# Kernel tuning notes

Measured on AMD Instinct MI355X. Metric: run time of the kernel, lower is better.

The kernel has to match this reference:

```python
import jax, jax.numpy as jnp
import numpy as np

B, N, NE = 16, 96, 256
ATOM, EDIM, HID, LAT, HEADS = 128, 16, 128, 128, 4
HD = LAT // HEADS
RBF, CUT, ZEMB, MAXZ = 16, 5.0, 32, 100
MUL0_IN, MUL1_IN = 64, 32      # irreps_node = 64x0e + 32x1o (dim 160)
MUL0_OUT, MUL1_OUT = 32, 16    # out irreps  = 32x0e + 16x1o (dim 80)
NODE_DIM = MUL0_IN + 3 * MUL1_IN
OUT_DIM = MUL0_OUT + 3 * MUL1_OUT
E_ATT = 1024
WNUM = MUL0_IN*MUL0_OUT + MUL0_IN*MUL1_OUT + MUL1_IN*MUL1_OUT + MUL1_IN*MUL0_OUT  # 4608


def _mlp3(x, w1, b1, w2, b2, w3, b3):
    x = jax.nn.silu(x @ w1 + b1)
    x = jax.nn.silu(x @ w2 + b2)
    return x @ w3 + b3


def setup_inputs() -> dict:
    key = jax.random.key(0)
    ks = jax.random.split(key, 40)
    s = 0.05  # scale params so deep MLP activations stay numerically sane
    d = {}
    d['h'] = jax.random.normal(ks[0], (B, N, ATOM), jnp.float32)
    d['h_full'] = jax.random.normal(ks[1], (B, N, NODE_DIM), jnp.float32)
    d['e_feat'] = jax.random.normal(ks[2], (NE, EDIM), jnp.float32)
    d['att_dist'] = jax.random.uniform(ks[3], (E_ATT,), jnp.float32)
    d['att_vec'] = jax.random.normal(ks[4], (E_ATT, 3), jnp.float32)
    d['z_emb_table'] = jax.random.normal(ks[5], (MAXZ + 1, ZEMB), jnp.float32) * s
    d['rw1'] = jax.random.normal(ks[6], (ZEMB + 1 + RBF, HID), jnp.float32) * s
    d['rb1'] = jnp.zeros((HID,), jnp.float32)
    d['rw2'] = jax.random.normal(ks[7], (HID, WNUM), jnp.float32) * s
    d['rb2'] = jnp.zeros((WNUM,), jnp.float32)
    d['ew1'] = jax.random.normal(ks[8], (EDIM, HID), jnp.float32) * s
    d['eb1'] = jnp.zeros((HID,), jnp.float32)
    d['ew2'] = jax.random.normal(ks[9], (HID, MUL0_OUT + MUL1_OUT), jnp.float32) * s
    d['eb2'] = jnp.zeros((MUL0_OUT + MUL1_OUT,), jnp.float32)
    d['qw1'] = jax.random.normal(ks[10], (ATOM + EDIM, HID), jnp.float32) * s
    d['qb1'] = jnp.zeros((HID,), jnp.float32)
    d['qw2'] = jax.random.normal(ks[11], (HID, HID), jnp.float32) * s
    d['qb2'] = jnp.zeros((HID,), jnp.float32)
    d['qw3'] = jax.random.normal(ks[12], (HID, LAT), jnp.float32) * s
    d['qb3'] = jnp.zeros((LAT,), jnp.float32)
    d['kw1'] = jax.random.normal(ks[13], (ATOM + ZEMB + 1 + RBF, HID), jnp.float32) * s
    d['kb1'] = jnp.zeros((HID,), jnp.float32)
    d['kw2'] = jax.random.normal(ks[14], (HID, HID), jnp.float32) * s
    d['kb2'] = jnp.zeros((HID,), jnp.float32)
    d['kw3'] = jax.random.normal(ks[15], (HID, LAT), jnp.float32) * s
    d['kb3'] = jnp.zeros((LAT,), jnp.float32)
    d['ow1'] = jax.random.normal(ks[16], (MUL0_OUT + MUL1_OUT, HID), jnp.float32) * s
    d['ob1'] = jnp.zeros((HID,), jnp.float32)
    d['ow2'] = jax.random.normal(ks[17], (HID, HID), jnp.float32) * s
    d['ob2'] = jnp.zeros((HID,), jnp.float32)
    d['ow3'] = jax.random.normal(ks[18], (HID, LAT), jnp.float32) * s
    d['ob3'] = jnp.zeros((LAT,), jnp.float32)
    d['z'] = jax.random.randint(ks[19], (B, N), 0, MAXZ)
    d['mask'] = jnp.ones((B, N), bool)
    d['absorber_index'] = jax.random.randint(ks[20], (B,), 0, N)
    d['att_dst'] = jnp.arange(E_ATT)  # unique flat indices into B*N
    return d


def reference(h, h_full, e_feat, att_dist, att_vec, z_emb_table,
              rw1, rb1, rw2, rb2, ew1, eb1, ew2, eb2,
              qw1, qb1, qw2, qb2, qw3, qb3,
              kw1, kb1, kw2, kb2, kw3, kb3,
              ow1, ob1, ow2, ob2, ow3, ob3,
              z, mask, absorber_index, att_dst):
    Bz, Na, Hd = h.shape
    F = Bz * Na
    nE = e_feat.shape[0]
    # scatter edge data into flat (B*N) atom slots
    am_flat = jnp.zeros((F,), bool).at[att_dst].set(True)
    d_flat = jnp.zeros((F,), h.dtype).at[att_dst].set(att_dist)
    v_flat = jnp.zeros((F, 3), h.dtype).at[att_dst].set(att_vec)
    att_mask = am_flat.reshape(Bz, Na) & mask
    # spherical harmonics (lmax=1, component normalization): Y0 = 1, Y1 = sqrt(3)*unit_vec
    un = v_flat / jnp.maximum(jnp.linalg.norm(v_flat, axis=-1, keepdims=True), 1e-8)
    y1 = jnp.sqrt(3.0) * un
    # Gaussian RBF on absorber->atom distance
    mu = jnp.linspace(0.0, CUT, RBF)
    delta = CUT / (RBF - 1)
    rbf = jnp.exp(-(d_flat[:, None] - mu) ** 2 / (2.0 * delta * delta))  # (F, RBF)
    zr = z_emb_table[z]                      # (B, N, ZEMB)
    zr_flat = zr.reshape(F, -1)
    is_abs = jnp.zeros((Bz, Na), h.dtype).at[jnp.arange(Bz), absorber_index].set(1.0)
    # radial MLP -> per-edge tensor-product weights
    w_in = jnp.concatenate([zr_flat, is_abs.reshape(F, 1), rbf], -1)
    tpw = jax.nn.silu(w_in @ rw1 + rb1) @ rw2 + rb2  # (F, WNUM)
    s1 = MUL0_IN * MUL0_OUT
    s2 = s1 + MUL0_IN * MUL1_OUT
    s3 = s2 + MUL1_IN * MUL1_OUT
    w00 = tpw[:, :s1].reshape(F, MUL0_IN, MUL0_OUT)   # 0e x 0e -> 0e
    w01 = tpw[:, s1:s2].reshape(F, MUL0_IN, MUL1_OUT) # 0e x 1o -> 1o
    w10 = tpw[:, s2:s3].reshape(F, MUL1_IN, MUL1_OUT) # 1o x 0e -> 1o
    w11 = tpw[:, s3:].reshape(F, MUL1_IN, MUL0_OUT)   # 1o x 1o -> 0e
    hf = h_full.reshape(F, -1)
    x0 = hf[:, :MUL0_IN]
    x1 = hf[:, MUL0_IN:].reshape(F, MUL1_IN, 3)
    alpha = 1.0 / jnp.sqrt(jnp.float32(MUL0_IN + MUL1_IN))  # path fan-in normalization
    c = 1.0 / jnp.sqrt(3.0)                                  # wigner-3j coeff for l=1 couplings
    out0 = alpha * (jnp.einsum('fi,fio->fo', x0, w00)
                    + c * jnp.einsum('fim,fm,fio->fo', x1, y1, w11))
    out1 = alpha * c * (jnp.einsum('fi,fm,fio->fom', x0, y1, w01)
                        + jnp.einsum('fim,fio->fom', x1, w10))
    v_irrep = jnp.concatenate([out0, out1.reshape(F, 3 * MUL1_OUT)], -1)  # (F, OUT_DIM)
    # cosine cutoff envelope + edge mask
    env = jnp.where(d_flat < CUT, 0.5 * (jnp.cos(jnp.pi * d_flat / CUT) + 1.0), 0.0)
    v_irrep = v_irrep * (am_flat.astype(h.dtype) * env)[:, None]
    # energy-conditioned per-irrep-channel modulation
    gates = jax.nn.silu(e_feat @ ew1 + eb1) @ ew2 + eb2  # (nE, 48)
    g_exp = jnp.concatenate([gates[:, :MUL0_OUT],
                             jnp.repeat(gates[:, MUL0_OUT:], 3, axis=-1)], -1)  # (nE, OUT_DIM)
    v_mod = (v_irrep[:, None, :] * g_exp[None]).reshape(Bz, Na, nE, OUT_DIM)
    # invariant multi-head scoring
    h_abs = h[jnp.arange(Bz), absorber_index]  # (B, H)
    q_in = jnp.concatenate([jnp.broadcast_to(h_abs[:, None], (Bz, nE, Hd)),
                            jnp.broadcast_to(e_feat[None], (Bz, nE, EDIM))], -1)
    q = _mlp3(q_in, qw1, qb1, qw2, qb2, qw3, qb3)  # (B, nE, LAT)
    atom_static = jnp.concatenate([h, zr, is_abs[..., None], rbf.reshape(Bz, Na, RBF)], -1)
    k = _mlp3(atom_static, kw1, kb1, kw2, kb2, kw3, kb3)  # (B, N, LAT)
    qh = q.reshape(Bz, nE, HEADS, HD)
    kh = k.reshape(Bz, Na, HEADS, HD)
    scores = (jnp.einsum('behd,bnhd->benh', qh, kh) * (HD ** -0.5)).mean(-1)  # (B, nE, N)
    m = att_mask[:, None, :]
    scores = jnp.where(m, scores, -1e9)
    attn = jax.nn.softmax(scores, axis=2) * m.astype(h.dtype)
    attn = attn / jnp.maximum(attn.sum(2, keepdims=True), 1e-8)
    out_irrep = jnp.einsum('ben,bnec->bec', attn, v_mod)  # (B, nE, OUT_DIM)
    # invariants: scalars + vector norms
    scal = out_irrep[..., :MUL0_OUT]
    vec = out_irrep[..., MUL0_OUT:].reshape(Bz, nE, MUL1_OUT, 3)
    inv = jnp.concatenate([scal, jnp.sqrt(jnp.sum(vec * vec, -1) + 1e-12)], -1)
    return _mlp3(inv, ow1, ob1, ow2, ob2, ow3, ob3)  # (B, nE, LAT)
```

## Files before the change

### kernel.cpp

```cpp
#include <hip/hip_runtime.h>
#include <hip/hip_fp16.h>
#include <math.h>

#define BB 16
#define NN 96
#define NE 256
#define FF (BB*NN)
#define ATOM 128
#define EDIM 16
#define HID 128
#define LAT 128
#define RBFN 16
#define CUTOFF 5.0f
#define ZEMB 32
#define E_ATT 1024
#define M0I 64
#define M1I 32
#define M0O 32
#define M1O 16
#define NODE_DIM 160
#define OUT_DIM 80
#define INVD 48
#define WNUM 4608
#define SEG1 2048
#define SEG2 3072
#define SEG3 3584

#define EDGE_BLKS (E_ATT/4)
#define EC_BLKS 16
#define HABS_BLKS 2
#define GATE_BLKS 16
#define TRANS_BLKS 144
#define PREP_BLKS 1
#define STAGE1_BLKS (EDGE_BLKS + EC_BLKS + HABS_BLKS + GATE_BLKS + TRANS_BLKS + PREP_BLKS)

#define MFMA_BLKS (36*16)
#define MQ_BLKS (MFMA_BLKS + 512)

#define SCORE_BLKS 128
#define ST_BLKS (SCORE_BLKS + 512)

typedef _Float16 half8_t __attribute__((ext_vector_type(8)));
typedef float float4v __attribute__((ext_vector_type(4)));

__device__ __forceinline__ float silu_f(float x) { return x / (1.0f + expf(-x)); }

__global__ __launch_bounds__(256) void k_stage1(
    const float* __restrict__ h, const float* __restrict__ z_emb, const int* __restrict__ z,
    const int* __restrict__ absorber, const float* __restrict__ e_feat,
    const int* __restrict__ att_dst, const float* __restrict__ att_dist,
    const float* __restrict__ att_vec,
    const float* __restrict__ rw1, const float* __restrict__ rb1,
    const float* __restrict__ kw1, const float* __restrict__ kb1,
    const float* __restrict__ kw2, const float* __restrict__ kb2,
    const float* __restrict__ kw3, const float* __restrict__ kb3,
    const float* __restrict__ qw1,
    const float* __restrict__ ew1, const float* __restrict__ eb1,
    const float* __restrict__ ew2, const float* __restrict__ eb2,
    const float* __restrict__ rw2,
    __half* __restrict__ hiddenH, float* __restrict__ kmatw,
    float* __restrict__ ecw, float* __restrict__ habs1w, float* __restrict__ gexp,
    __half* __restrict__ rw2T,
    int* __restrict__ inv, float* __restrict__ y1E, float* __restrict__ envE)
{
    __shared__ float smem[3488];
    int blk = blockIdx.x;
    int t = threadIdx.x;

    if (blk < EDGE_BLKS) {
        float (*sin1)[184] = (float(*)[184])smem;
        float (*l1S)[128]  = (float(*)[128])(smem + 736);
        float (*l2S)[128]  = (float(*)[128])(smem + 736 + 512);
        int w = t >> 6;
        int c = t & 63;
        int e = blk*4 + w;
        int f = att_dst[e];
        int b = f / NN, nn = f - b*NN;
        float d = att_dist[e];
        {
            float2 hv = *(const float2*)&h[f*ATOM + 2*c];
            sin1[w][2*c] = hv.x; sin1[w][2*c + 1] = hv.y;
        }
        if (c < ZEMB) sin1[w][ATOM + c] = z_emb[z[f]*ZEMB + c];
        if (c >= 32 && c < 48) {
            int j = c - 32;
            const float delta = CUTOFF / (RBFN - 1);
            float diff = d - j*delta;
            sin1[w][ATOM + ZEMB + 1 + j] = expf(-diff*diff / (2.0f*delta*delta));
        }
        if (c == 48) sin1[w][ATOM + ZEMB] = (absorber[b] == nn) ? 1.0f : 0.0f;
        __syncthreads();
        int c2 = 2*c;
        {
            float2 a0 = *(const float2*)&rb1[c2];
            float2 a1 = make_float2(0.f, 0.f);
            #pragma unroll 8
            for (int i = 0; i < 48; i += 2) {
                float x0v = sin1[w][ATOM + i], x1v = sin1[w][ATOM + i + 1];
                float2 w0 = *(const float2*)&rw1[i*HID + c2];
                float2 w1 = *(const float2*)&rw1[(i+1)*HID + c2];
                a0.x += x0v*w0.x; a0.y += x0v*w0.y;
                a1.x += x1v*w1.x; a1.y += x1v*w1.y;
            }
            {
                float x0v = sin1[w][ATOM + 48];
                float2 w0 = *(const float2*)&rw1[48*HID + c2];
                a0.x += x0v*w0.x; a0.y += x0v*w0.y;
            }
            *(__half2*)&hiddenH[e*HID + c2] =
                __floats2half2_rn(silu_f(a0.x + a1.x), silu_f(a0.y + a1.y));
        }
        {
            float2 a0 = *(const float2*)&kb1[c2];
            float2 a1 = make_float2(0.f, 0.f);
            #pragma unroll 8
            for (int i = 0; i < 176; i += 2) {
                float x0v = sin1[w][i], x1v = sin1[w][i + 1];
                float2 w0 = *(const float2*)&kw1[i*HID + c2];
                float2 w1 = *(const float2*)&kw1[(i+1)*HID + c2];
                a0.x += x0v*w0.x; a0.y += x0v*w0.y;
                a1.x += x1v*w1.x; a1.y += x1v*w1.y;
            }
            {
                float x0v = sin1[w][176];
                float2 w0 = *(const float2*)&kw1[176*HID + c2];
                a0.x += x0v*w0.x; a0.y += x0v*w0.y;
            }
            l1S[w][c2] = silu_f(a0.x + a1.x); l1S[w][c2+1] = silu_f(a0.y + a1.y);
        }
        __syncthreads();
        {
            float2 a0 = *(const float2*)&kb2[c2];
            float2 a1 = make_float2(0.f, 0.f);
            #pragma unroll 8
            for (int i = 0; i < HID; i += 2) {
                float x0v = l1S[w][i], x1v = l1S[w][i + 1];
                float2 w0 = *(const float2*)&kw2[i*HID + c2];
                float2 w1 = *(const float2*)&kw2[(i+1)*HID + c2];
                a0.x += x0v*w0.x; a0.y += x0v*w0.y;
                a1.x += x1v*w1.x; a1.y += x1v*w1.y;
            }
            l2S[w][c2] = silu_f(a0.x + a1.x); l2S[w][c2+1] = silu_f(a0.y + a1.y);
        }
        __syncthreads();
        {
            float2 a0 = *(const float2*)&kb3[c2];
            float2 a1 = make_float2(0.f, 0.f);
            #pragma unroll 8
            for (int i = 0; i < HID; i += 2) {
                float x0v = l2S[w][i], x1v = l2S[w][i + 1];
                float2 w0 = *(const float2*)&kw3[i*HID + c2];
                float2 w1 = *(const float2*)&kw3[(i+1)*HID + c2];
                a0.x += x0v*w0.x; a0.y += x0v*w0.y;
                a1.x += x1v*w1.x; a1.y += x1v*w1.y;
            }
            float2 o; o.x = a0.x + a1.x; o.y = a0.y + a1.y;
            *(float2*)&kmatw[f*HID + c2] = o;
        }
    } else if (blk < EDGE_BLKS + EC_BLKS) {
        float (*ef)[16] = (float(*)[16])smem;
        int e0 = (blk - EDGE_BLKS) * 16;
        { int e = t >> 4, i = t & 15; ef[e][i] = e_feat[(e0 + e)*EDIM + i]; }
        __syncthreads();
        int r = t >> 4, c0 = (t & 15)*8;
        float4 a0 = make_float4(0,0,0,0), a1 = a0;
        #pragma unroll
        for (int i = 0; i < EDIM; i++) {
            float a = ef[r][i];
            float4 w0 = *(const float4*)&qw1[(ATOM + i)*HID + c0];
            float4 w1 = *(const float4*)&qw1[(ATOM + i)*HID + c0 + 4];
            a0.x += a*w0.x; a0.y += a*w0.y; a0.z += a*w0.z; a0.w += a*w0.w;
            a1.x += a*w1.x; a1.y += a*w1.y; a1.z += a*w1.z; a1.w += a*w1.w;
        }
        *(float4*)&ecw[(e0 + r)*HID + c0] = a0;
        *(float4*)&ecw[(e0 + r)*HID + c0 + 4] = a1;
    } else if (blk < EDGE_BLKS + EC_BLKS + HABS_BLKS) {
        float (*hr)[128] = (float(*)[128])smem;
        int b0 = (blk - EDGE_BLKS - EC_BLKS) * 8;
        {
            int r = t >> 5, i4 = t & 31;
            int b = b0 + r;
            int a = absorber[b];
            *(float4*)&hr[r][i4*4] = *(const float4*)&h[(b*NN + a)*ATOM + i4*4];
        }
        __syncthreads();
        int r = t >> 5, c0 = (t & 31)*4;
        float4 a0 = make_float4(0,0,0,0), a1 = a0;
        #pragma unroll 8
        for (int i = 0; i < ATOM; i += 2) {
            float x0v = hr[r][i], x1v = hr[r][i+1];
            float4 w0 = *(const float4*)&qw1[i*HID + c0];
            float4 w1 = *(const float4*)&qw1[(i+1)*HID + c0];
            a0.x += x0v*w0.x; a0.y += x0v*w0.y; a0.z += x0v*w0.z; a0.w += x0v*w0.w;
            a1.x += x1v*w1.x; a1.y += x1v*w1.y; a1.z += x1v*w1.z; a1.w += x1v*w1.w;
        }
        float4 o;
        o.x = a0.x + a1.x; o.y = a0.y + a1.y; o.z = a0.z + a1.z; o.w = a0.w + a1.w;
        *(float4*)&habs1w[(b0 + r)*HID + c0] = o;
    } else if (blk < EDGE_BLKS + EC_BLKS + HABS_BLKS + GATE_BLKS) {
        float (*ef)[16]   = (float(*)[16])smem;
        float (*l1g)[128] = (float(*)[128])(smem + 256);
        float (*gg)[48]   = (float(*)[48])(smem + 256 + 2048);
        int e0 = (blk - EDGE_BLKS - EC_BLKS - HABS_BLKS) * 16;
        { int e = t >> 4, i = t & 15; ef[e][i] = e_feat[(e0 + e)*EDIM + i]; }
        __syncthreads();
        int r = t >> 4, c0 = (t & 15)*8;
        {
            float4 a0 = *(const float4*)&eb1[c0];
            float4 a1 = *(const float4*)&eb1[c0 + 4];
            #pragma unroll
            for (int i = 0; i < EDIM; i++) {
                float a = ef[r][i];
                float4 w0 = *(const float4*)&ew1[i*HID + c0];
                float4 w1 = *(const float4*)&ew1[i*HID + c0 + 4];
                a0.x += a*w0.x; a0.y += a*w0.y; a0.z += a*w0.z; a0.w += a*w0.w;
                a1.x += a*w1.x; a1.y += a*w1.y; a1.z += a*w1.z; a1.w += a*w1.w;
            }
            l1g[r][c0]   = silu_f(a0.x); l1g[r][c0+1] = silu_f(a0.y);
            l1g[r][c0+2] = silu_f(a0.z); l1g[r][c0+3] = silu_f(a0.w);
            l1g[r][c0+4] = silu_f(a1.x); l1g[r][c0+5] = silu_f(a1.y);
            l1g[r][c0+6] = silu_f(a1.z); l1g[r][c0+7] = silu_f(a1.w);
        }
        __syncthreads();
        for (int u = t; u < 16*48; u += 256) {
            int e = u / 48, j = u - 48*(u/48);
            float acc = eb2[j];
            #pragma unroll 4
            for (int i = 0; i < HID; i++) acc += l1g[e][i]*ew2[i*48 + j];
            gg[e][j] = acc;
        }
        __syncthreads();
        for (int u = t; u < 16*80; u += 256) {
            int e = u / 80, cc = u - 80*(u/80);
            gexp[(e0 + e)*OUT_DIM + cc] = (cc < M0O) ? gg[e][cc] : gg[e][M0O + (cc - M0O)/3];
        }
    } else if (blk < EDGE_BLKS + EC_BLKS + HABS_BLKS + GATE_BLKS + TRANS_BLKS) {
        __half* lds = (__half*)smem;
        int tb = blk - (EDGE_BLKS + EC_BLKS + HABS_BLKS + GATE_BLKS);
        int nt = tb % 72, kt = tb / 72;
        int n0 = nt*64, k0 = kt*64;
        for (int p = 0; p < 16; p++) {
            int idx = t + 256*p;
            int kk = idx >> 6, nn = idx & 63;
            lds[nn*66 + kk] = __float2half(rw2[(k0+kk)*WNUM + n0+nn]);
        }
        __syncthreads();
        for (int p = 0; p < 16; p++) {
            int idx = t + 256*p;
            int nn = idx >> 6, kk = idx & 63;
            rw2T[(n0+nn)*HID + k0+kk] = lds[nn*66 + kk];
        }
    } else {
        for (int p = 0; p < 6; p++) inv[t + 256*p] = -1;
        for (int p = 0; p < 4; p++) {
            int e = t + 256*p;
            float d = att_dist[e];
            envE[e] = (d < CUTOFF) ? 0.5f*(cosf(3.14159265358979323846f*d/CUTOFF) + 1.0f) : 0.0f;
            float vx = att_vec[3*e], vy = att_vec[3*e+1], vz = att_vec[3*e+2];
            float nrm = sqrtf(vx*vx + vy*vy + vz*vz);
            float is = 1.0f / fmaxf(nrm, 1e-8f);
            const float s3 = 1.7320508075688772f;
            y1E[3*e]   = s3*vx*is;
            y1E[3*e+1] = s3*vy*is;
            y1E[3*e+2] = s3*vz*is;
        }
        __syncthreads();
        for (int p = 0; p < 4; p++) { int e = t + 256*p; inv[att_dst[e]] = e; }
    }
}

__global__ __launch_bounds__(256) void k_mq(
    const __half* __restrict__ hiddenH, const __half* __restrict__ rw2T,
    const float* __restrict__ rb2,
    const float* __restrict__ habs1, const float* __restrict__ ec, const float* __restrict__ qb1,
    const float* __restrict__ qw2, const float* __restrict__ qb2,
    const float* __restrict__ qw3, const float* __restrict__ qb3,
    __half* __restrict__ tpwE, float* __restrict__ qmat)
{
    __shared__ __align__(16) char smemraw[17408];
    int blk = blockIdx.x;
    int t = threadIdx.x;
    if (blk < MFMA_BLKS) {
        int colTile = blk % 36;
        int rowGrp  = blk / 36;
        int wv = t >> 6;
        int lane = t & 63;
        int m0 = (rowGrp*4 + wv) * 16;
        int n0 = colTile * 128;
        int mrow = lane & 15, quad = lane >> 4;
        __half* cS = (__half*)smemraw + wv * (16*136);
        const _Float16* hp = (const _Float16*)hiddenH + (m0 + mrow)*HID + quad*8;
        half8_t af[4];
        #pragma unroll
        for (int kc = 0; kc < 4; kc++) af[kc] = *(const half8_t*)(hp + kc*32);
        #pragma unroll
        for (int nt = 0; nt < 8; nt++) {
            const _Float16* bp = (const _Float16*)rw2T + (n0 + nt*16 + mrow)*HID + quad*8;
            float4v acc = {0.f, 0.f, 0.f, 0.f};
            #pragma unroll
            for (int kc = 0; kc < 4; kc++) {
                half8_t bf = *(const half8_t*)(bp + kc*32);
                acc = __builtin_amdgcn_mfma_f32_16x16x32_f16(af[kc], bf, acc, 0, 0, 0);
            }
            float bias = rb2[n0 + nt*16 + mrow];
            #pragma unroll
            for (int r = 0; r < 4; r++)
                cS[(quad*4 + r)*136 + nt*16 + mrow] = __float2half(acc[r] + bias);
        }
        #pragma unroll
        for (int p = 0; p < 4; p++) {
            int chunk = lane + 64*p;
            int row = chunk >> 4, c8 = (chunk & 15)*8;
            float4 v = *(float4*)&cS[row*136 + c8];
            *(float4*)&tpwE[(long)(m0 + row)*WNUM + n0 + c8] = v;
        }
    } else {
        float* l1S = (float*)smemraw;
        float* l2S = (float*)smemraw + 1024;
        int r0 = (blk - MFMA_BLKS) * 8;
        for (int p = 0; p < 4; p++) {
            int idx = t + 256*p;
            int rr = idx >> 7, i = idx & 127;
            int be = r0 + rr; int b = be >> 8; int e = be & 255;
            l1S[rr*128 + i] = silu_f(habs1[b*HID + i] + ec[e*HID + i] + qb1[i]);
        }
        __syncthreads();
        int r = t >> 5, c0 = (t & 31)*4;
        {
            float4 a0 = *(const float4*)&qb2[c0];
            float4 a1 = make_float4(0,0,0,0);
            #pragma unroll 8
            for (int i = 0; i < HID; i += 2) {
                float x0v = l1S[r*128 + i], x1v = l1S[r*128 + i+1];
                float4 w0 = *(const float4*)&qw2[i*HID + c0];
                float4 w1 = *(const float4*)&qw2[(i+1)*HID + c0];
                a0.x += x0v*w0.x; a0.y += x0v*w0.y; a0.z += x0v*w0.z; a0.w += x0v*w0.w;
                a1.x += x1v*w1.x; a1.y += x1v*w1.y; a1.z += x1v*w1.z; a1.w += x1v*w1.w;
            }
            l2S[r*128 + c0]   = silu_f(a0.x + a1.x); l2S[r*128 + c0+1] = silu_f(a0.y + a1.y);
            l2S[r*128 + c0+2] = silu_f(a0.z + a1.z); l2S[r*128 + c0+3] = silu_f(a0.w + a1.w);
        }
        __syncthreads();
        {
            float4 a0 = *(const float4*)&qb3[c0];
            float4 a1 = make_float4(0,0,0,0);
            #pragma unroll 8
            for (int i = 0; i < HID; i += 2) {
                float x0v = l2S[r*128 + i], x1v = l2S[r*128 + i+1];
                float4 w0 = *(const float4*)&qw3[i*HID + c0];
                float4 w1 = *(const float4*)&qw3[(i+1)*HID + c0];
                a0.x += x0v*w0.x; a0.y += x0v*w0.y; a0.z += x0v*w0.z; a0.w += x0v*w0.w;
                a1.x += x1v*w1.x; a1.y += x1v*w1.y; a1.z += x1v*w1.z; a1.w += x1v*w1.w;
            }
            float4 o;
            o.x = a0.x + a1.x; o.y = a0.y + a1.y; o.z = a0.z + a1.z; o.w = a0.w + a1.w;
            *(float4*)&qmat[(r0 + r)*LAT + c0] = o;
        }
    }
}

__global__ __launch_bounds__(256) void k_st(
    const float* __restrict__ qmat, const float* __restrict__ kmat, const int* __restrict__ inv,
    const float* __restrict__ h_full, const __half* __restrict__ tpwE,
    const int* __restrict__ att_dst,
    const float* __restrict__ envE, const float* __restrict__ y1E,
    float* __restrict__ scoresW, float* __restrict__ virr)
{
    __shared__ float smem[8544];
    int blk = blockIdx.x;
    int t = threadIdx.x;
    if (blk < SCORE_BLKS) {
        int b  = blk >> 3;
        int e0 = (blk & 7) * 32;
        float (*Qs)[132] = (float(*)[132])smem;
        float (*Kt)[132] = (float(*)[132])(smem + 32*132);
        float* mS = smem + 2*32*132;
        for (int p = 0; p < 4; p++) {
            int idx = t + 256*p; int e = idx >> 5, i4 = idx & 31;
            *(float4*)&Qs[e][i4*4] = *(const float4*)&qmat[(b*NE + e0 + e)*LAT + i4*4];
        }
        if (t < NN) mS[t] = ((unsigned)inv[b*NN + t] < E_ATT) ? 1.0f : 0.0f;
        int te = t >> 5, tn = t & 31;
        float acc[4][3] = {};
        for (int nt = 0; nt < 3; nt++) {
            __syncthreads();
            for (int p = 0; p < 4; p++) {
                int idx = t + 256*p; int n = idx >> 5, i4 = idx & 31;
                *(float4*)&Kt[n][i4*4] = *(const float4*)&kmat[(b*NN + nt*32 + n)*LAT + i4*4];
            }
            __syncthreads();
            for (int i = 0; i < LAT; i++) {
                float bv = Kt[tn][i];
                acc[0][nt] += Qs[te*4 + 0][i]*bv;
                acc[1][nt] += Qs[te*4 + 1][i]*bv;
                acc[2][nt] += Qs[te*4 + 2][i]*bv;
                acc[3][nt] += Qs[te*4 + 3][i]*bv;
            }
        }
        const float scale = 0.04419417382415922f;
        #pragma unroll
        for (int j = 0; j < 4; j++)
            #pragma unroll
            for (int jj = 0; jj < 3; jj++) {
                int n = tn + 32*jj;
                float s = (mS[n] != 0.f) ? acc[j][jj]*scale : -1e9f;
                scoresW[((b*NE) + e0 + te*4 + j)*NN + n] = s;
            }
    } else {
        int sub = t >> 7, tt = t & 127;
        int e = (blk - SCORE_BLKS)*2 + sub;
        int f = att_dst[e];
        float* x0  = smem + sub*256;
        float* x1f = smem + sub*256 + 64;
        float* xy  = smem + sub*256 + 160;
        float* y1s = smem + sub*256 + 192;
        const float* hf = h_full + f*NODE_DIM;
        if (tt < M0I) x0[tt] = hf[tt];
        if (tt < M1I*3) x1f[tt] = hf[M0I + tt];
        if (tt < 3) y1s[tt] = y1E[3*e + tt];
        __syncthreads();
        if (tt < M1I) xy[tt] = x1f[3*tt]*y1s[0] + x1f[3*tt+1]*y1s[1] + x1f[3*tt+2]*y1s[2];
        __syncthreads();
        float scale = envE[e];
        const __half* w = tpwE + (long)e*WNUM;
        const float alpha = 0.10206207261596575f;
        const float cc = 0.5773502691896258f;
        if (tt < M0O) {
            float t00 = 0.f, t11 = 0.f;
            #pragma unroll 4
            for (int i = 0; i < M0I; i++) t00 += x0[i]*__half2float(w[i*M0O + tt]);
            #pragma unroll 4
            for (int i = 0; i < M1I; i++) t11 += xy[i]*__half2float(w[SEG3 + i*M0O + tt]);
            virr[f*OUT_DIM + tt] = alpha*(t00 + cc*t11)*scale;
        } else if (tt < M0O + 3*M1O) {
            int idx = tt - M0O; int o = idx/3, m = idx - 3*o;
            float t01 = 0.f, t10 = 0.f;
            #pragma unroll 4
            for (int i = 0; i < M0I; i++) t01 += x0[i]*__half2float(w[SEG1 + i*M1O + o]);
            #pragma unroll 4
            for (int i = 0; i < M1I; i++) t10 += x1f[i*3 + m]*__half2float(w[SEG2 + i*M1O + o]);
            virr[f*OUT_DIM + tt] = alpha*cc*(t01*y1s[m] + t10)*scale;
        }
    }
}

__global__ __launch_bounds__(256) void k_attf(
    const float* __restrict__ scoresW, const int* __restrict__ inv,
    const float* __restrict__ virr, const float* __restrict__ gexp,
    const float* __restrict__ ow1, const float* __restrict__ ob1,
    const float* __restrict__ ow2, const float* __restrict__ ob2,
    const float* __restrict__ ow3, const float* __restrict__ ob3,
    float* __restrict__ out)
{
    int b  = blockIdx.x >> 5;
    int e0 = (blockIdx.x & 31) * 8;
    int t = threadIdx.x;
    __shared__ float aS[8][100];
    __shared__ float gS[8][84];
    __shared__ float ocS[8][84];
    __shared__ float mS[NN];
    __shared__ float inS[8][INVD];
    __shared__ float l1S[8][HID];
    __shared__ float l2S[8][HID];

    for (int p = 0; p < 3; p++) {
        int idx = t + 256*p;
        int el = idx / NN, n = idx - NN*(idx/NN);
        aS[el][n] = scoresW[((b*NE) + e0 + el)*NN + n];
    }
    if (t < 160) {
        int el = t / 20, c4 = t - 20*(t/20);
        *(float4*)&gS[el][c4*4] = *(const float4*)&gexp[(e0 + el)*OUT_DIM + c4*4];
    }
    if (t < NN) mS[t] = ((unsigned)inv[b*NN + t] < E_ATT) ? 1.0f : 0.0f;
    __syncthreads();

    {
        int el = t >> 5;
        int ng = t & 31;
        float s0 = aS[el][ng], s1 = aS[el][ng + 32], s2 = aS[el][ng + 64];
        float m0 = mS[ng], m1 = mS[ng + 32], m2 = mS[ng + 64];
        float mx = fmaxf(s0, fmaxf(s1, s2));
        #pragma unroll
        for (int off = 1; off < 32; off <<= 1) mx = fmaxf(mx, __shfl_xor(mx, off));
        float e0v = expf(s0 - mx), e1v = expf(s1 - mx), e2v = expf(s2 - mx);
        float sm = e0v + e1v + e2v;
        #pragma unroll
        for (int off = 1; off < 32; off <<= 1) sm += __shfl_xor(sm, off);
        float r = 1.0f / sm;
        float p0 = m0*e0v*r, p1 = m1*e1v*r, p2 = m2*e2v*r;
        float ss = p0 + p1 + p2;
        #pragma unroll
        for (int off = 1; off < 32; off <<= 1) ss += __shfl_xor(ss, off);
        float is = 1.0f / fmaxf(ss, 1e-8f);
        aS[el][ng]      = p0*is;
        aS[el][ng + 32] = p1*is;
        aS[el][ng + 64] = p2*is;
    }
    __syncthreads();

    if (t < 160) {
        int el = t / 20, c4 = t - 20*(t/20);
        const float* vp = virr + (long)b*NN*OUT_DIM + c4*4;
        float4 acc = make_float4(0,0,0,0);
        #pragma unroll 4
        for (int n = 0; n < NN; n++) {
            float a = aS[el][n];
            float4 v = *(const float4*)&vp[n*OUT_DIM];
            acc.x += a*v.x; acc.y += a*v.y; acc.z += a*v.z; acc.w += a*v.w;
        }
        float4 g = *(float4*)&gS[el][c4*4];
        float4 o; o.x = acc.x*g.x; o.y = acc.y*g.y; o.z = acc.z*g.z; o.w = acc.w*g.w;
        *(float4*)&ocS[el][c4*4] = o;
    }
    __syncthreads();

    for (int u = t; u < 8*INVD; u += 256) {
        int el = u / INVD, j = u - INVD*(u/INVD);
        float val;
        if (j < M0O) val = ocS[el][j];
        else {
            int o = j - M0O;
            float x = ocS[el][M0O + 3*o], y = ocS[el][M0O + 3*o + 1], zz = ocS[el][M0O + 3*o + 2];
            val = sqrtf(x*x + y*y + zz*zz + 1e-12f);
        }
        inS[el][j] = val;
    }
    __syncthreads();

    int r = t >> 5, c0 = (t & 31)*4;
    {
        float4 a0 = *(const float4*)&ob1[c0];
        float4 a1 = make_float4(0,0,0,0);
        #pragma unroll 8
        for (int i = 0; i < INVD; i += 2) {
            float x0v = inS[r][i], x1v = inS[r][i+1];
            float4 w0 = *(const float4*)&ow1[i*HID + c0];
            float4 w1 = *(const float4*)&ow1[(i+1)*HID + c0];
            a0.x += x0v*w0.x; a0.y += x0v*w0.y; a0.z += x0v*w0.z; a0.w += x0v*w0.w;
            a1.x += x1v*w1.x; a1.y += x1v*w1.y; a1.z += x1v*w1.z; a1.w += x1v*w1.w;
        }
        l1S[r][c0]   = silu_f(a0.x + a1.x); l1S[r][c0+1] = silu_f(a0.y + a1.y);
        l1S[r][c0+2] = silu_f(a0.z + a1.z); l1S[r][c0+3] = silu_f(a0.w + a1.w);
    }
    __syncthreads();
    {
        float4 a0 = *(const float4*)&ob2[c0];
        float4 a1 = make_float4(0,0,0,0);
        #pragma unroll 8
        for (int i = 0; i < HID; i += 2) {
            float x0v = l1S[r][i], x1v = l1S[r][i+1];
            float4 w0 = *(const float4*)&ow2[i*HID + c0];
            float4 w1 = *(const float4*)&ow2[(i+1)*HID + c0];
            a0.x += x0v*w0.x; a0.y += x0v*w0.y; a0.z += x0v*w0.z; a0.w += x0v*w0.w;
            a1.x += x1v*w1.x; a1.y += x1v*w1.y; a1.z += x1v*w1.z; a1.w += x1v*w1.w;
        }
        l2S[r][c0]   = silu_f(a0.x + a1.x); l2S[r][c0+1] = silu_f(a0.y + a1.y);
        l2S[r][c0+2] = silu_f(a0.z + a1.z); l2S[r][c0+3] = silu_f(a0.w + a1.w);
    }
    __syncthreads();
    {
        float4 a0 = *(const float4*)&ob3[c0];
        float4 a1 = make_float4(0,0,0,0);
        #pragma unroll 8
        for (int i = 0; i < HID; i += 2) {
            float x0v = l2S[r][i], x1v = l2S[r][i+1];
            float4 w0 = *(const float4*)&ow3[i*HID + c0];
            float4 w1 = *(const float4*)&ow3[(i+1)*HID + c0];
            a0.x += x0v*w0.x; a0.y += x0v*w0.y; a0.z += x0v*w0.z; a0.w += x0v*w0.w;
            a1.x += x1v*w1.x; a1.y += x1v*w1.y; a1.z += x1v*w1.z; a1.w += x1v*w1.w;
        }
        float4 o;
        o.x = a0.x + a1.x; o.y = a0.y + a1.y; o.z = a0.z + a1.z; o.w = a0.w + a1.w;
        *(float4*)&out[((b*NE + e0) + r)*LAT + c0] = o;
    }
}

extern "C" void kernel_launch(void* const* d_in, const int* in_sizes, int n_in,
                              void* d_out, int out_size, void* d_ws, size_t ws_size,
                              hipStream_t stream) {
    const float* h        = (const float*)d_in[0];
    const float* h_full   = (const float*)d_in[1];
    const float* e_feat   = (const float*)d_in[2];
    const float* att_dist = (const float*)d_in[3];
    const float* att_vec  = (const float*)d_in[4];
    const float* z_emb    = (const float*)d_in[5];
    const float* rw1 = (const float*)d_in[6];  const float* rb1 = (const float*)d_in[7];
    const float* rw2 = (const float*)d_in[8];  const float* rb2 = (const float*)d_in[9];
    const float* ew1 = (const float*)d_in[10]; const float* eb1 = (const float*)d_in[11];
    const float* ew2 = (const float*)d_in[12]; const float* eb2 = (const float*)d_in[13];
    const float* qw1 = (const float*)d_in[14]; const float* qb1 = (const float*)d_in[15];
    const float* qw2 = (const float*)d_in[16]; const float* qb2 = (const float*)d_in[17];
    const float* qw3 = (const float*)d_in[18]; const float* qb3 = (const float*)d_in[19];
    const float* kw1 = (const float*)d_in[20]; const float* kb1 = (const float*)d_in[21];
    const float* kw2 = (const float*)d_in[22]; const float* kb2 = (const float*)d_in[23];
    const float* kw3 = (const float*)d_in[24]; const float* kb3 = (const float*)d_in[25];
    const float* ow1 = (const float*)d_in[26]; const float* ob1 = (const float*)d_in[27];
    const float* ow2 = (const float*)d_in[28]; const float* ob2 = (const float*)d_in[29];
    const float* ow3 = (const float*)d_in[30]; const float* ob3 = (const float*)d_in[31];
    const int* z        = (const int*)d_in[32];
    const int* absorber = (const int*)d_in[34];
    const int* att_dst  = (const int*)d_in[35];

    float* ws = (float*)d_ws;
    int*   inv     = (int*)ws;
    float* y1E     = ws + 1536;
    float* envE    = ws + 4608;
    float* kmat    = ws + 5632;
    float* qmat    = ws + 202240;
    float* gexp    = ws + 726528;
    float* virr    = ws + 747008;
    float* habs1   = ws + 869888;
    float* ec      = ws + 871936;
    float* scoresW = ws + 904704;
    __half* tpwE   = (__half*)(ws + 1297920);
    __half* rw2T   = (__half*)(ws + 3657216);
    __half* hiddenH= (__half*)(ws + 3952128);

    float* out = (float*)d_out;

    k_stage1<<<STAGE1_BLKS, 256, 0, stream>>>(h, z_emb, z, absorber, e_feat,
                                              att_dst, att_dist, att_vec,
                                              rw1, rb1, kw1, kb1, kw2, kb2, kw3, kb3,
                                              qw1, ew1, eb1, ew2, eb2, rw2,
                                              hiddenH, kmat, ec, habs1, gexp, rw2T,
                                              inv, y1E, envE);
    k_mq<<<MQ_BLKS, 256, 0, stream>>>(hiddenH, rw2T, rb2, habs1, ec, qb1,
                                      qw2, qb2, qw3, qb3, tpwE, qmat);
    k_st<<<ST_BLKS, 256, 0, stream>>>(qmat, kmat, inv, h_full, tpwE, att_dst,
                                      envE, y1E, scoresW, virr);
    k_attf<<<BB*32, 256, 0, stream>>>(scoresW, inv, virr, gexp,
                                      ow1, ob1, ow2, ob2, ow3, ob3, out);
}
```

Measured before the change: 237.5 us.

## Fuse four stage kernels into one persistent kernel with grid barriers

Replaces the four separate kernel launches with a single persistent kernel of 512 blocks. Each block loops over the work units of each former stage, and stages are separated by an atomic-counter grid barrier, with a tiny init kernel resetting the counter. The intent is to remove inter-kernel launch gaps and tail drain between the stages. In exchange it relies on all 512 blocks being co-resident (launch_bounds 256,2 plus about 34 KB of shared memory), which risks deadlock if they are not, and it adds spin-wait barrier overhead and possibly lower per-block occupancy.

Result: slower. 494.0 us (+108.0%).

```diff
diff --git a/kernel.cpp b/kernel.cpp
--- a/kernel.cpp
+++ b/kernel.cpp
@@ -31,604 +31,639 @@
 #define HABS_BLKS 2
 #define GATE_BLKS 16
 #define TRANS_BLKS 144
-#define PREP_BLKS 1
-#define STAGE1_BLKS (EDGE_BLKS + EC_BLKS + HABS_BLKS + GATE_BLKS + TRANS_BLKS + PREP_BLKS)
-
-#define MFMA_BLKS (36*16)
-#define MQ_BLKS (MFMA_BLKS + 512)
-
-#define SCORE_BLKS 128
-#define ST_BLKS (SCORE_BLKS + 512)
+#define STAGE1_UNITS (EDGE_BLKS + EC_BLKS + HABS_BLKS + GATE_BLKS + TRANS_BLKS + 1)
+
+#define MFMA_UNITS (36*16)
+#define MQ_UNITS (MFMA_UNITS + 512)
+
+#define SCORE_UNITS 128
+#define ST_UNITS (SCORE_UNITS + 512)
+
+#define ATT_UNITS 512
+
+#define GRID_BLKS 512
+#define SMEM_BYTES 34304
 
 typedef _Float16 half8_t __attribute__((ext_vector_type(8)));
 typedef float float4v __attribute__((ext_vector_type(4)));
 
 __device__ __forceinline__ float silu_f(float x) { return x / (1.0f + expf(-x)); }
 
-__global__ __launch_bounds__(256) void k_stage1(
-    const float* __restrict__ h, const float* __restrict__ z_emb, const int* __restrict__ z,
-    const int* __restrict__ absorber, const float* __restrict__ e_feat,
-    const int* __restrict__ att_dst, const float* __restrict__ att_dist,
-    const float* __restrict__ att_vec,
-    const float* __restrict__ rw1, const float* __restrict__ rb1,
-    const float* __restrict__ kw1, const float* __restrict__ kb1,
-    const float* __restrict__ kw2, const float* __restrict__ kb2,
-    const float* __restrict__ kw3, const float* __restrict__ kb3,
-    const float* __restrict__ qw1,
-    const float* __restrict__ ew1, const float* __restrict__ eb1,
-    const float* __restrict__ ew2, const float* __restrict__ eb2,
-    const float* __restrict__ rw2,
-    __half* __restrict__ hiddenH, float* __restrict__ kmatw,
-    float* __restrict__ ecw, float* __restrict__ habs1w, float* __restrict__ gexp,
-    __half* __restrict__ rw2T,
-    int* __restrict__ inv, float* __restrict__ y1E, float* __restrict__ envE)
+__device__ __forceinline__ void grid_barrier(int* cnt, int target) {
+    __syncthreads();
+    if (threadIdx.x == 0) {
+        __threadfence();
+        atomicAdd(cnt, 1);
+        while (__hip_atomic_load(cnt, __ATOMIC_RELAXED, __HIP_MEMORY_SCOPE_AGENT) < target) {
+            __builtin_amdgcn_s_sleep(2);
+        }
+    }
+    __syncthreads();
+    __threadfence();
+}
+
+struct Params {
+    const float *h, *h_full, *e_feat, *att_dist, *att_vec, *z_emb;
+    const float *rw1, *rb1, *rw2, *rb2;
+    const float *ew1, *eb1, *ew2, *eb2;
+    const float *qw1, *qb1, *qw2, *qb2, *qw3, *qb3;
+    const float *kw1, *kb1, *kw2, *kb2, *kw3, *kb3;
+    const float *ow1, *ob1, *ow2, *ob2, *ow3, *ob3;
+    const int *z, *absorber, *att_dst;
+    __half *hiddenH; float *kmat; float *ec; float *habs1; float *gexp;
+    __half *rw2T; int *inv; float *y1E; float *envE;
+    float *qmat; float *scoresW; __half *tpwE; float *virr;
+    int *bar;
+    float *out;
+};
+
+__global__ void k_init(int* bar) {
+    if (threadIdx.x == 0) bar[0] = 0;
+}
+
+__global__ __launch_bounds__(256, 2) void k_mega(Params p)
 {
-    __shared__ float smem[3488];
-    int blk = blockIdx.x;
-    int t = threadIdx.x;
-
-    if (blk < EDGE_BLKS) {
-        float (*sin1)[184] = (float(*)[184])smem;
-        float (*l1S)[128]  = (float(*)[128])(smem + 736);
-        float (*l2S)[128]  = (float(*)[128])(smem + 736 + 512);
-        int w = t >> 6;
-        int c = t & 63;
-        int e = blk*4 + w;
-        int f = att_dst[e];
-        int b = f / NN, nn = f - b*NN;
-        float d = att_dist[e];
-        {
-            float2 hv = *(const float2*)&h[f*ATOM + 2*c];
-            sin1[w][2*c] = hv.x; sin1[w][2*c + 1] = hv.y;
-        }
-        if (c < ZEMB) sin1[w][ATOM + c] = z_emb[z[f]*ZEMB + c];
-        if (c >= 32 && c < 48) {
-            int j = c - 32;
-            const float delta = CUTOFF / (RBFN - 1);
-            float diff = d - j*delta;
-            sin1[w][ATOM + ZEMB + 1 + j] = expf(-diff*diff / (2.0f*delta*delta));
-        }
-        if (c == 48) sin1[w][ATOM + ZEMB] = (absorber[b] == nn) ? 1.0f : 0.0f;
-        __syncthreads();
-        int c2 = 2*c;
-        {
-            float2 a0 = *(const float2*)&rb1[c2];
-            float2 a1 = make_float2(0.f, 0.f);
-            #pragma unroll 8
-            for (int i = 0; i < 48; i += 2) {
-                float x0v = sin1[w][ATOM + i], x1v = sin1[w][ATOM + i + 1];
-                float2 w0 = *(const float2*)&rw1[i*HID + c2];
-                float2 w1 = *(const float2*)&rw1[(i+1)*HID + c2];
-                a0.x += x0v*w0.x; a0.y += x0v*w0.y;
-                a1.x += x1v*w1.x; a1.y += x1v*w1.y;
-            }
-            {
-                float x0v = sin1[w][ATOM + 48];
-                float2 w0 = *(const float2*)&rw1[48*HID + c2];
-                a0.x += x0v*w0.x; a0.y += x0v*w0.y;
-            }
-            *(__half2*)&hiddenH[e*HID + c2] =
-                __floats2half2_rn(silu_f(a0.x + a1.x), silu_f(a0.y + a1.y));
-        }
-        {
-            float2 a0 = *(const float2*)&kb1[c2];
-            float2 a1 = make_float2(0.f, 0.f);
-            #pragma unroll 8
-            for (int i = 0; i < 176; i += 2) {
-                float x0v = sin1[w][i], x1v = sin1[w][i + 1];
-                float2 w0 = *(const float2*)&kw1[i*HID + c2];
-                float2 w1 = *(const float2*)&kw1[(i+1)*HID + c2];
-                a0.x += x0v*w0.x; a0.y += x0v*w0.y;
-                a1.x += x1v*w1.x; a1.y += x1v*w1.y;
-            }
-            {
-                float x0v = sin1[w][176];
-                float2 w0 = *(const float2*)&kw1[176*HID + c2];
-                a0.x += x0v*w0.x; a0.y += x0v*w0.y;
-            }
-            l1S[w][c2] = silu_f(a0.x + a1.x); l1S[w][c2+1] = silu_f(a0.y + a1.y);
-        }
-        __syncthreads();
-        {
-            float2 a0 = *(const float2*)&kb2[c2];
-            float2 a1 = make_float2(0.f, 0.f);
-            #pragma unroll 8
-            for (int i = 0; i < HID; i += 2) {
-                float x0v = l1S[w][i], x1v = l1S[w][i + 1];
-                float2 w0 = *(const float2*)&kw2[i*HID + c2];
-                float2 w1 = *(const float2*)&kw2[(i+1)*HID + c2];
-                a0.x += x0v*w0.x; a0.y += x0v*w0.y;
-                a1.x += x1v*w1.x; a1.y += x1v*w1.y;
-            }
-            l2S[w][c2] = silu_f(a0.x + a1.x); l2S[w][c2+1] = silu_f(a0.y + a1.y);
-        }
-        __syncthreads();
-        {
-            float2 a0 = *(const float2*)&kb3[c2];
-            float2 a1 = make_float2(0.f, 0.f);
-            #pragma unroll 8
-            for (int i = 0; i < HID; i += 2) {
-                float x0v = l2S[w][i], x1v = l2S[w][i + 1];
-                float2 w0 = *(const float2*)&kw3[i*HID + c2];
-                float2 w1 = *(const float2*)&kw3[(i+1)*HID + c2];
-                a0.x += x0v*w0.x; a0.y += x0v*w0.y;
-                a1.x += x1v*w1.x; a1.y += x1v*w1.y;
-            }
-            float2 o; o.x = a0.x + a1.x; o.y = a0.y + a1.y;
-            *(float2*)&kmatw[f*HID + c2] = o;
-        }
-    } else if (blk < EDGE_BLKS + EC_BLKS) {
-        float (*ef)[16] = (float(*)[16])smem;
-        int e0 = (blk - EDGE_BLKS) * 16;
-        { int e = t >> 4, i = t & 15; ef[e][i] = e_feat[(e0 + e)*EDIM + i]; }
-        __syncthreads();
-        int r = t >> 4, c0 = (t & 15)*8;
-        float4 a0 = make_float4(0,0,0,0), a1 = a0;
-        #pragma unroll
-        for (int i = 0; i < EDIM; i++) {
-            float a = ef[r][i];
-            float4 w0 = *(const float4*)&qw1[(ATOM + i)*HID + c0];
-            float4 w1 = *(const float4*)&qw1[(ATOM + i)*HID + c0 + 4];
-            a0.x += a*w0.x; a0.y += a*w0.y; a0.z += a*w0.z; a0.w += a*w0.w;
-            a1.x += a*w1.x; a1.y += a*w1.y; a1.z += a*w1.z; a1.w += a*w1.w;
-        }
-        *(float4*)&ecw[(e0 + r)*HID + c0] = a0;
-        *(float4*)&ecw[(e0 + r)*HID + c0 + 4] = a1;
-    } else if (blk < EDGE_BLKS + EC_BLKS + HABS_BLKS) {
-        float (*hr)[128] = (float(*)[128])smem;
-        int b0 = (blk - EDGE_BLKS - EC_BLKS) * 8;
-        {
-            int r = t >> 5, i4 = t & 31;
-            int b = b0 + r;
-            int a = absorber[b];
-            *(float4*)&hr[r][i4*4] = *(const float4*)&h[(b*NN + a)*ATOM + i4*4];
-        }
-        __syncthreads();
-        int r = t >> 5, c0 = (t & 31)*4;
-        float4 a0 = make_float4(0,0,0,0), a1 = a0;
-        #pragma unroll 8
-        for (int i = 0; i < ATOM; i += 2) {
-            float x0v = hr[r][i], x1v = hr[r][i+1];
-            float4 w0 = *(const float4*)&qw1[i*HID + c0];
-            float4 w1 = *(const float4*)&qw1[(i+1)*HID + c0];
-            a0.x += x0v*w0.x; a0.y += x0v*w0.y; a0.z += x0v*w0.z; a0.w += x0v*w0.w;
-            a1.x += x1v*w1.x; a1.y += x1v*w1.y; a1.z += x1v*w1.z; a1.w += x1v*w1.w;
-        }
-        float4 o;
-        o.x = a0.x + a1.x; o.y = a0.y + a1.y; o.z = a0.z + a1.z; o.w = a0.w + a1.w;
-        *(float4*)&habs1w[(b0 + r)*HID + c0] = o;
-    } else if (blk < EDGE_BLKS + EC_BLKS + HABS_BLKS + GATE_BLKS) {
-        float (*ef)[16]   = (float(*)[16])smem;
-        float (*l1g)[128] = (float(*)[128])(smem + 256);
-        float (*gg)[48]   = (float(*)[48])(smem + 256 + 2048);
-        int e0 = (blk - EDGE_BLKS - EC_BLKS - HABS_BLKS) * 16;
-        { int e = t >> 4, i = t & 15; ef[e][i] = e_feat[(e0 + e)*EDIM + i]; }
-        __syncthreads();
-        int r = t >> 4, c0 = (t & 15)*8;
-        {
-            float4 a0 = *(const float4*)&eb1[c0];
-            float4 a1 = *(const float4*)&eb1[c0 + 4];
+    __shared__ __align__(16) char smemraw[SMEM_BYTES];
+    float* smem = (float*)smemraw;
+    const int t = threadIdx.x;
+    const int blk = blockIdx.x;
+
+    const float* __restrict__ h        = p.h;
+    const float* __restrict__ h_full   = p.h_full;
+    const float* __restrict__ e_feat   = p.e_feat;
+    const float* __restrict__ att_dist = p.att_dist;
+    const float* __restrict__ att_vec  = p.att_vec;
+    const float* __restrict__ z_emb    = p.z_emb;
+    const float* __restrict__ rw1 = p.rw1; const float* __restrict__ rb1 = p.rb1;
+    const float* __restrict__ rw2 = p.rw2; const float* __restrict__ rb2 = p.rb2;
+    const float* __restrict__ ew1 = p.ew1; const float* __restrict__ eb1 = p.eb1;
+    const float* __restrict__ ew2 = p.ew2; const float* __restrict__ eb2 = p.eb2;
+    const float* __restrict__ qw1 = p.qw1; const float* __restrict__ qb1 = p.qb1;
+    const float* __restrict__ qw2 = p.qw2; const float* __restrict__ qb2 = p.qb2;
+    const float* __restrict__ qw3 = p.qw3; const float* __restrict__ qb3 = p.qb3;
+    const float* __restrict__ kw1 = p.kw1; const float* __restrict__ kb1 = p.kb1;
+    const float* __restrict__ kw2 = p.kw2; const float* __restrict__ kb2 = p.kb2;
+    const float* __restrict__ kw3 = p.kw3; const float* __restrict__ kb3 = p.kb3;
+    const float* __restrict__ ow1 = p.ow1; const float* __restrict__ ob1 = p.ob1;
+    const float* __restrict__ ow2 = p.ow2; const float* __restrict__ ob2 = p.ob2;
+    const float* __restrict__ ow3 = p.ow3; const float* __restrict__ ob3 = p.ob3;
+    const int* __restrict__ z        = p.z;
+    const int* __restrict__ absorber = p.absorber;
+    const int* __restrict__ att_dst  = p.att_dst;
+    __half* __restrict__ hiddenH = p.hiddenH;
+    float*  __restrict__ kmat    = p.kmat;
+    float*  __restrict__ ec      = p.ec;
+    float*  __restrict__ habs1   = p.habs1;
+    float*  __restrict__ gexp    = p.gexp;
+    __half* __restrict__ rw2T    = p.rw2T;
+    int*    __restrict__ inv     = p.inv;
+    float*  __restrict__ y1E     = p.y1E;
+    float*  __restrict__ envE    = p.envE;
+    float*  __restrict__ qmat    = p.qmat;
+    float*  __restrict__ scoresW = p.scoresW;
+    __half* __restrict__ tpwE    = p.tpwE;
+    float*  __restrict__ virr    = p.virr;
+    float*  __restrict__ out     = p.out;
+    int* bar = p.bar;
+
+    for (int u = blk; u < STAGE1_UNITS; u += GRID_BLKS) {
+        if (u < EDGE_BLKS) {
+            float (*sin1)[184] = (float(*)[184])smem;
+            float (*l1S)[128]  = (float(*)[128])(smem + 736);
+            float (*l2S)[128]  = (float(*)[128])(smem + 736 + 512);
+            int w = t >> 6;
+            int c = t & 63;
+            int e = u*4 + w;
+            int f = att_dst[e];
+            int b = f / NN, nn = f - b*NN;
+            float d = att_dist[e];
+            {
+                float2 hv = *(const float2*)&h[f*ATOM + 2*c];
+                sin1[w][2*c] = hv.x; sin1[w][2*c + 1] = hv.y;
+            }
+            if (c < ZEMB) sin1[w][ATOM + c] = z_emb[z[f]*ZEMB + c];
+            if (c >= 32 && c < 48) {
+                int j = c - 32;
+                const float delta = CUTOFF / (RBFN - 1);
+                float diff = d - j*delta;
+                sin1[w][ATOM + ZEMB + 1 + j] = expf(-diff*diff / (2.0f*delta*delta));
+            }
+            if (c == 48) sin1[w][ATOM + ZEMB] = (absorber[b] == nn) ? 1.0f : 0.0f;
+            __syncthreads();
+            int c2 = 2*c;
+            {
+                float2 a0 = *(const float2*)&rb1[c2];
+                float2 a1 = make_float2(0.f, 0.f);
+                #pragma unroll 8
+                for (int i = 0; i < 48; i += 2) {
+                    float x0v = sin1[w][ATOM + i], x1v = sin1[w][ATOM + i + 1];
+                    float2 w0 = *(const float2*)&rw1[i*HID + c2];
+                    float2 w1 = *(const float2*)&rw1[(i+1)*HID + c2];
+                    a0.x += x0v*w0.x; a0.y += x0v*w0.y;
+                    a1.x += x1v*w1.x; a1.y += x1v*w1.y;
+                }
+                {
+                    float x0v = sin1[w][ATOM + 48];
+                    float2 w0 = *(const float2*)&rw1[48*HID + c2];
+                    a0.x += x0v*w0.x; a0.y += x0v*w0.y;
+                }
+                *(__half2*)&hiddenH[e*HID + c2] =
+                    __floats2half2_rn(silu_f(a0.x + a1.x), silu_f(a0.y + a1.y));
+            }
+            {
+                float2 a0 = *(const float2*)&kb1[c2];
+                float2 a1 = make_float2(0.f, 0.f);
+                #pragma unroll 8
+                for (int i = 0; i < 176; i += 2) {
+                    float x0v = sin1[w][i], x1v = sin1[w][i + 1];
+                    float2 w0 = *(const float2*)&kw1[i*HID + c2];
+                    float2 w1 = *(const float2*)&kw1[(i+1)*HID + c2];
+                    a0.x += x0v*w0.x; a0.y += x0v*w0.y;
+                    a1.x += x1v*w1.x; a1.y += x1v*w1.y;
+                }
+                {
+                    float x0v = sin1[w][176];
+                    float2 w0 = *(const float2*)&kw1[176*HID + c2];
+                    a0.x += x0v*w0.x; a0.y += x0v*w0.y;
+                }
+                l1S[w][c2] = silu_f(a0.x + a1.x); l1S[w][c2+1] = silu_f(a0.y + a1.y);
+            }
+            __syncthreads();
+            {
+                float2 a0 = *(const float2*)&kb2[c2];
+                float2 a1 = make_float2(0.f, 0.f);
+                #pragma unroll 8
+                for (int i = 0; i < HID; i += 2) {
+                    float x0v = l1S[w][i], x1v = l1S[w][i + 1];
+                    float2 w0 = *(const float2*)&kw2[i*HID + c2];
+                    float2 w1 = *(const float2*)&kw2[(i+1)*HID + c2];
+                    a0.x += x0v*w0.x; a0.y += x0v*w0.y;
+                    a1.x += x1v*w1.x; a1.y += x1v*w1.y;
+                }
+                l2S[w][c2] = silu_f(a0.x + a1.x); l2S[w][c2+1] = silu_f(a0.y + a1.y);
+            }
+            __syncthreads();
+            {
+                float2 a0 = *(const float2*)&kb3[c2];
+                float2 a1 = make_float2(0.f, 0.f);
+                #pragma unroll 8
+                for (int i = 0; i < HID; i += 2) {
+                    float x0v = l2S[w][i], x1v = l2S[w][i + 1];
+                    float2 w0 = *(const float2*)&kw3[i*HID + c2];
+                    float2 w1 = *(const float2*)&kw3[(i+1)*HID + c2];
+                    a0.x += x0v*w0.x; a0.y += x0v*w0.y;
+                    a1.x += x1v*w1.x; a1.y += x1v*w1.y;
+                }
+                float2 o; o.x = a0.x + a1.x; o.y = a0.y + a1.y;
+                *(float2*)&kmat[f*HID + c2] = o;
+            }
+        } else if (u < EDGE_BLKS + EC_BLKS) {
+            float (*ef)[16] = (float(*)[16])smem;
+            int e0 = (u - EDGE_BLKS) * 16;
+            { int e = t >> 4, i = t & 15; ef[e][i] = e_feat[(e0 + e)*EDIM + i]; }
+            __syncthreads();
+            int r = t >> 4, c0 = (t & 15)*8;
+            float4 a0 = make_float4(0,0,0,0), a1 = a0;
             #pragma unroll
             for (int i = 0; i < EDIM; i++) {
                 float a = ef[r][i];
-                float4 w0 = *(const float4*)&ew1[i*HID + c0];
-                float4 w1 = *(const float4*)&ew1[i*HID + c0 + 4];
+                float4 w0 = *(const float4*)&qw1[(ATOM + i)*HID + c0];
+                float4 w1 = *(const float4*)&qw1[(ATOM + i)*HID + c0 + 4];
                 a0.x += a*w0.x; a0.y += a*w0.y; a0.z += a*w0.z; a0.w += a*w0.w;
                 a1.x += a*w1.x; a1.y += a*w1.y; a1.z += a*w1.z; a1.w += a*w1.w;
             }
-            l1g[r][c0]   = silu_f(a0.x); l1g[r][c0+1] = silu_f(a0.y);
-            l1g[r][c0+2] = silu_f(a0.z); l1g[r][c0+3] = silu_f(a0.w);
-            l1g[r][c0+4] = silu_f(a1.x); l1g[r][c0+5] = silu_f(a1.y);
-            l1g[r][c0+6] = silu_f(a1.z); l1g[r][c0+7] = silu_f(a1.w);
-        }
-        __syncthreads();
-        for (int u = t; u < 16*48; u += 256) {
-            int e = u / 48, j = u - 48*(u/48);
-            float acc = eb2[j];
+            *(float4*)&ec[(e0 + r)*HID + c0] = a0;
+            *(float4*)&ec[(e0 + r)*HID + c0 + 4] = a1;
+        } else if (u < EDGE_BLKS + EC_BLKS + HABS_BLKS) {
+            float (*hr)[128] = (float(*)[128])smem;
+            int b0 = (u - EDGE_BLKS - EC_BLKS) * 8;
+            {
+                int r = t >> 5, i4 = t & 31;
+                int b = b0 + r;
+                int a = absorber[b];
+                *(float4*)&hr[r][i4*4] = *(const float4*)&h[(b*NN + a)*ATOM + i4*4];
+            }
+            __syncthreads();
+            int r = t >> 5, c0 = (t & 31)*4;
+            float4 a0 = make_float4(0,0,0,0), a1 = a0;
+            #pragma unroll 8
+            for (int i = 0; i < ATOM; i += 2) {
+                float x0v = hr[r][i], x1v = hr[r][i+1];
+                float4 w0 = *(const float4*)&qw1[i*HID + c0];
+                float4 w1 = *(const float4*)&qw1[(i+1)*HID + c0];
+                a0.x += x0v*w0.x; a0.y += x0v*w0.y; a0.z += x0v*w0.z; a0.w += x0v*w0.w;
+                a1.x += x1v*w1.x; a1.y += x1v*w1.y; a1.z += x1v*w1.z; a1.w += x1v*w1.w;
+            }
+            float4 o;
+            o.x = a0.x + a1.x; o.y = a0.y + a1.y; o.z = a0.z + a1.z; o.w = a0.w + a1.w;
+            *(float4*)&habs1[(b0 + r)*HID + c0] = o;
+        } else if (u < EDGE_BLKS + EC_BLKS + HABS_BLKS + GATE_BLKS) {
+            float (*ef)[16]   = (float(*)[16])smem;
+            float (*l1g)[128] = (float(*)[128])(smem + 256);
+            float (*gg)[48]   = (float(*)[48])(smem + 256 + 2048);
+            int e0 = (u - EDGE_BLKS - EC_BLKS - HABS_BLKS) * 16;
+            { int e = t >> 4, i = t & 15; ef[e][i] = e_feat[(e0 + e)*EDIM + i]; }
+            __syncthreads();
+            int r = t >> 4, c0 = (t & 15)*8;
+            {
+                float4 a0 = *(const float4*)&eb1[c0];
+                float4 a1 = *(const float4*)&eb1[c0 + 4];
+                #pragma unroll
+                for (int i = 0; i < EDIM; i++) {
+                    float a = ef[r][i];
+                    float4 w0 = *(const float4*)&ew1[i*HID + c0];
+                    float4 w1 = *(const float4*)&ew1[i*HID + c0 + 4];
+                    a0.x += a*w0.x; a0.y += a*w0.y; a0.z += a*w0.z; a0.w += a*w0.w;
+                    a1.x += a*w1.x; a1.y += a*w1.y; a1.z += a*w1.z; a1.w += a*w1.w;
+                }
+                l1g[r][c0]   = silu_f(a0.x); l1g[r][c0+1] = silu_f(a0.y);
+                l1g[r][c0+2] = silu_f(a0.z); l1g[r][c0+3] = silu_f(a0.w);
+                l1g[r][c0+4] = silu_f(a1.x); l1g[r][c0+5] = silu_f(a1.y);
+                l1g[r][c0+6] = silu_f(a1.z); l1g[r][c0+7] = silu_f(a1.w);
+            }
+            __syncthreads();
+            for (int uu = t; uu < 16*48; uu += 256) {
+                int e = uu / 48, j = uu - 48*(uu/48);
+                float acc = eb2[j];
+                #pragma unroll 4
+                for (int i = 0; i < HID; i++) acc += l1g[e][i]*ew2[i*48 + j];
+                gg[e][j] = acc;
+            }
+            __syncthreads();
+            for (int uu = t; uu < 16*80; uu += 256) {
+                int e = uu / 80, cc = uu - 80*(uu/80);
+                gexp[(e0 + e)*OUT_DIM + cc] = (cc < M0O) ? gg[e][cc] : gg[e][M0O + (cc - M0O)/3];
+            }
+        } else if (u < EDGE_BLKS + EC_BLKS + HABS_BLKS + GATE_BLKS + TRANS_BLKS) {
+            __half* lds = (__half*)smem;
+            int tb = u - (EDGE_BLKS + EC_BLKS + HABS_BLKS + GATE_BLKS);
+            int nt = tb % 72, kt = tb / 72;
+            int n0 = nt*64, k0 = kt*64;
+            for (int pp = 0; pp < 16; pp++) {
+                int idx = t + 256*pp;
+                int kk = idx >> 6, nn = idx & 63;
+                lds[nn*66 + kk] = __float2half(rw2[(k0+kk)*WNUM + n0+nn]);
+            }
+            __syncthreads();
+            for (int pp = 0; pp < 16; pp++) {
+                int idx = t + 256*pp;
+                int nn = idx >> 6, kk = idx & 63;
+                rw2T[(n0+nn)*HID + k0+kk] = lds[nn*66 + kk];
+            }
+        } else {
+            for (int pp = 0; pp < 6; pp++) inv[t + 256*pp] = -1;
+            for (int pp = 0; pp < 4; pp++) {
+                int e = t + 256*pp;
+                float d = att_dist[e];
+                envE[e] = (d < CUTOFF) ? 0.5f*(cosf(3.14159265358979323846f*d/CUTOFF) + 1.0f) : 0.0f;
+                float vx = att_vec[3*e], vy = att_vec[3*e+1], vz = att_vec[3*e+2];
+                float nrm = sqrtf(vx*vx + vy*vy + vz*vz);
+                float is = 1.0f / fmaxf(nrm, 1e-8f);
+                const float s3 = 1.7320508075688772f;
+                y1E[3*e]   = s3*vx*is;
+                y1E[3*e+1] = s3*vy*is;
+                y1E[3*e+2] = s3*vz*is;
+            }
+            __syncthreads();
+            for (int pp = 0; pp < 4; pp++) { int e = t + 256*pp; inv[att_dst[e]] = e; }
+        }
+    }
+
+    grid_barrier(bar, GRID_BLKS*1);
+
+    for (int u = blk; u < MQ_UNITS; u += GRID_BLKS) {
+        __syncthreads();
+        if (u < MFMA_UNITS) {
+            int colTile = u % 36;
+            int rowGrp  = u / 36;
+            int wv = t >> 6;
+            int lane = t & 63;
+            int m0 = (rowGrp*4 + wv) * 16;
+            int n0 = colTile * 128;
+            int mrow = lane & 15, quad = lane >> 4;
+            __half* cS = (__half*)smemraw + wv * (16*136);
+            const _Float16* hp = (const _Float16*)hiddenH + (m0 + mrow)*HID + quad*8;
+            half8_t af[4];
+            #pragma unroll
+            for (int kc = 0; kc < 4; kc++) af[kc] = *(const half8_t*)(hp + kc*32);
+            #pragma unroll
+            for (int nt = 0; nt < 8; nt++) {
+                const _Float16* bp = (const _Float16*)rw2T + (n0 + nt*16 + mrow)*HID + quad*8;
+                float4v acc = {0.f, 0.f, 0.f, 0.f};
+                #pragma unroll
+                for (int kc = 0; kc < 4; kc++) {
+                    half8_t bf = *(const half8_t*)(bp + kc*32);
+                    acc = __builtin_amdgcn_mfma_f32_16x16x32_f16(af[kc], bf, acc, 0, 0, 0);
+                }
+                float bias = rb2[n0 + nt*16 + mrow];
+                #pragma unroll
+                for (int r = 0; r < 4; r++)
+                    cS[(quad*4 + r)*136 + nt*16 + mrow] = __float2half(acc[r] + bias);
+            }
+            __syncthreads();
+            #pragma unroll
+            for (int pp = 0; pp < 4; pp++) {
+                int chunk = lane + 64*pp;
+                int row = chunk >> 4, c8 = (chunk & 15)*8;
+                float4 v = *(float4*)&cS[row*136 + c8];
+                *(float4*)&tpwE[(long)(m0 + row)*WNUM + n0 + c8] = v;
+            }
+        } else {
+            float* l1S = smem;
+            float* l2S = smem + 1024;
+            int r0 = (u - MFMA_UNITS) * 8;
+            for (int pp = 0; pp < 4; pp++) {
+                int idx = t + 256*pp;
+                int rr = idx >> 7, i = idx & 127;
+                int be = r0 + rr; int b = be >> 8; int e = be & 255;
+                l1S[rr*128 + i] = silu_f(habs1[b*HID + i] + ec[e*HID + i] + qb1[i]);
+            }
+            __syncthreads();
+            int r = t >> 5, c0 = (t & 31)*4;
+            {
+                float4 a0 = *(const float4*)&qb2[c0];
+                float4 a1 = make_float4(0,0,0,0);
+                #pragma unroll 8
+                for (int i = 0; i < HID; i += 2) {
+                    float x0v = l1S[r*128 + i], x1v = l1S[r*128 + i+1];
+                    float4 w0 = *(const float4*)&qw2[i*HID + c0];
+                    float4 w1 = *(const float4*)&qw2[(i+1)*HID + c0];
+                    a0.x += x0v*w0.x; a0.y += x0v*w0.y; a0.z += x0v*w0.z; a0.w += x0v*w0.w;
+                    a1.x += x1v*w1.x; a1.y += x1v*w1.y; a1.z += x1v*w1.z; a1.w += x1v*w1.w;
+                }
+                l2S[r*128 + c0]   = silu_f(a0.x + a1.x); l2S[r*128 + c0+1] = silu_f(a0.y + a1.y);
+                l2S[r*128 + c0+2] = silu_f(a0.z + a1.z); l2S[r*128 + c0+3] = silu_f(a0.w + a1.w);
+            }
+            __syncthreads();
+            {
+                float4 a0 = *(const float4*)&qb3[c0];
+                float4 a1 = make_float4(0,0,0,0);
+                #pragma unroll 8
+                for (int i = 0; i < HID; i += 2) {
+                    float x0v = l2S[r*128 + i], x1v = l2S[r*128 + i+1];
+                    float4 w0 = *(const float4*)&qw3[i*HID + c0];
+                    float4 w1 = *(const float4*)&qw3[(i+1)*HID + c0];
+                    a0.x += x0v*w0.x; a0.y += x0v*w0.y; a0.z += x0v*w0.z; a0.w += x0v*w0.w;
+                    a1.x += x1v*w1.x; a1.y += x1v*w1.y; a1.z += x1v*w1.z; a1.w += x1v*w1.w;
+                }
+                float4 o;
+                o.x = a0.x + a1.x; o.y = a0.y + a1.y; o.z = a0.z + a1.z; o.w = a0.w + a1.w;
+                *(float4*)&qmat[(r0 + r)*LAT + c0] = o;
+            }
+        }
+    }
+
+    grid_barrier(bar, GRID_BLKS*2);
+
+    for (int u = blk; u < ST_UNITS; u += GRID_BLKS) {
+        __syncthreads();
+        if (u < SCORE_UNITS) {
+            int b  = u >> 3;
+            int e0 = (u & 7) * 32;
+            float (*Qs)[132] = (float(*)[132])smem;
+            float (*Kt)[132] = (float(*)[132])(smem + 32*132);
+            float* mS = smem + 2*32*132;
+            for (int pp = 0; pp < 4; pp++) {
+                int idx = t + 256*pp; int e = idx >> 5, i4 = idx & 31;
+                *(float4*)&Qs[e][i4*4] = *(const float4*)&qmat[(b*NE + e0 + e)*LAT + i4*4];
+            }
+            if (t < NN) mS[t] = ((unsigned)inv[b*NN + t] < E_ATT) ? 1.0f : 0.0f;
+            int te = t >> 5, tn = t & 31;
+            float acc[4][3] = {};
+            for (int nt = 0; nt < 3; nt++) {
+                __syncthreads();
+                for (int pp = 0; pp < 4; pp++) {
+                    int idx = t + 256*pp; int n = idx >> 5, i4 = idx & 31;
+                    *(float4*)&Kt[n][i4*4] = *(const float4*)&kmat[(b*NN + nt*32 + n)*LAT + i4*4];
+                }
+                __syncthreads();
+                for (int i = 0; i < LAT; i++) {
+                    float bv = Kt[tn][i];
+                    acc[0][nt] += Qs[te*4 + 0][i]*bv;
+                    acc[1][nt] += Qs[te*4 + 1][i]*bv;
+                    acc[2][nt] += Qs[te*4 + 2][i]*bv;
+                    acc[3][nt] += Qs[te*4 + 3][i]*bv;
+                }
+            }
+            const float scale = 0.04419417382415922f;
+            #pragma unroll
+            for (int j = 0; j < 4; j++)
+                #pragma unroll
+                for (int jj = 0; jj < 3; jj++) {
+                    int n = tn + 32*jj;
+                    float s = (mS[n] != 0.f) ? acc[j][jj]*scale : -1e9f;
+                    scoresW[((b*NE) + e0 + te*4 + j)*NN + n] = s;
+                }
+        } else {
+            int sub = t >> 7, tt = t & 127;
+            int e = (u - SCORE_UNITS)*2 + sub;
+            int f = att_dst[e];
+            float* x0  = smem + sub*256;
+            float* x1f = smem + sub*256 + 64;
+            float* xy  = smem + sub*256 + 160;
+            float* y1s = smem + sub*256 + 192;
+            const float* hf = h_full + f*NODE_DIM;
+            if (tt < M0I) x0[tt] = hf[tt];
+            if (tt < M1I*3) x1f[tt] = hf[M0I + tt];
+            if (tt < 3) y1s[tt] = y1E[3*e + tt];
+            __syncthreads();
+            if (tt < M1I) xy[tt] = x1f[3*tt]*y1s[0] + x1f[3*tt+1]*y1s[1] + x1f[3*tt+2]*y1s[2];
+            __syncthreads();
+            float scale = envE[e];
+            const __half* w = tpwE + (long)e*WNUM;
+            const float alpha = 0.10206207261596575f;
+            const float cc = 0.5773502691896258f;
+            if (tt < M0O) {
+                float t00 = 0.f, t11 = 0.f;
+                #pragma unroll 4
+                for (int i = 0; i < M0I; i++) t00 += x0[i]*__half2float(w[i*M0O + tt]);
+                #pragma unroll 4
+                for (int i = 0; i < M1I; i++) t11 += xy[i]*__half2float(w[SEG3 + i*M0O + tt]);
+                virr[f*OUT_DIM + tt] = alpha*(t00 + cc*t11)*scale;
+            } else if (tt < M0O + 3*M1O) {
+                int idx = tt - M0O; int o = idx/3, m = idx - 3*o;
+                float t01 = 0.f, t10 = 0.f;
+                #pragma unroll 4
+                for (int i = 0; i < M0I; i++) t01 += x0[i]*__half2float(w[SEG1 + i*M1O + o]);
+                #pragma unroll 4
+                for (int i = 0; i < M1I; i++) t10 += x1f[i*3 + m]*__half2float(w[SEG2 + i*M1O + o]);
+                virr[f*OUT_DIM + tt] = alpha*cc*(t01*y1s[m] + t10)*scale;
+            }
+        }
+    }
+
+    grid_barrier(bar, GRID_BLKS*3);
+
+    for (int u = blk; u < ATT_UNITS; u += GRID_BLKS) {
+        int b  = u >> 5;
+        int e0 = (u & 31) * 8;
+        float (*aS)[100]  = (float(*)[100])smem;
+        float (*gS)[84]   = (float(*)[84])(smem + 800);
+        float (*ocS)[84]  = (float(*)[84])(smem + 1472);
+        float* mS         = smem + 2144;
+        float (*inS)[INVD] = (float(*)[INVD])(smem + 2240);
+        float (*l1S)[HID] = (float(*)[HID])(smem + 2624);
+        float (*l2S)[HID] = (float(*)[HID])(smem + 3648);
+
+        for (int pp = 0; pp < 3; pp++) {
+            int idx = t + 256*pp;
+            int el = idx / NN, n = idx - NN*(idx/NN);
+            aS[el][n] = scoresW[((b*NE) + e0 + el)*NN + n];
+        }
+        if (t < 160) {
+            int el = t / 20, c4 = t - 20*(t/20);
+            *(float4*)&gS[el][c4*4] = *(const float4*)&gexp[(e0 + el)*OUT_DIM + c4*4];
+        }
+        if (t < NN) mS[t] = ((unsigned)inv[b*NN + t] < E_ATT) ? 1.0f : 0.0f;
+        __syncthreads();
+
+        {
+            int el = t >> 5;
+            int ng = t & 31;
+            float s0 = aS[el][ng], s1 = aS[el][ng + 32], s2 = aS[el][ng + 64];
+            float m0 = mS[ng], m1 = mS[ng + 32], m2 = mS[ng + 64];
+            float mx = fmaxf(s0, fmaxf(s1, s2));
+            #pragma unroll
+            for (int off = 1; off < 32; off <<= 1) mx = fmaxf(mx, __shfl_xor(mx, off));
+            float e0v = expf(s0 - mx), e1v = expf(s1 - mx), e2v = expf(s2 - mx);
+            float sm = e0v + e1v + e2v;
+            #pragma unroll
+            for (int off = 1; off < 32; off <<= 1) sm += __shfl_xor(sm, off);
+            float r = 1.0f / sm;
+            float p0 = m0*e0v*r, p1 = m1*e1v*r, p2 = m2*e2v*r;
+            float ss = p0 + p1 + p2;
+            #pragma unroll
+            for (int off = 1; off < 32; off <<= 1) ss += __shfl_xor(ss, off);
+            float is = 1.0f / fmaxf(ss, 1e-8f);
+            aS[el][ng]      = p0*is;
+            aS[el][ng + 32] = p1*is;
+            aS[el][ng + 64] = p2*is;
+        }
+        __syncthreads();
+
+        if (t < 160) {
+            int el = t / 20, c4 = t - 20*(t/20);
+            const float* vp = virr + (long)b*NN*OUT_DIM + c4*4;
+            float4 acc = make_float4(0,0,0,0);
             #pragma unroll 4
-            for (int i = 0; i < HID; i++) acc += l1g[e][i]*ew2[i*48 + j];
-            gg[e][j] = acc;
-        }
-        __syncthreads();
-        for (int u = t; u < 16*80; u += 256) {
-            int e = u / 80, cc = u - 80*(u/80);
-            gexp[(e0 + e)*OUT_DIM + cc] = (cc < M0O) ? gg[e][cc] : gg[e][M0O + (cc - M0O)/3];
-        }
-    } else if (blk < EDGE_BLKS + EC_BLKS + HABS_BLKS + GATE_BLKS + TRANS_BLKS) {
-        __half* lds = (__half*)smem;
-        int tb = blk - (EDGE_BLKS + EC_BLKS + HABS_BLKS + GATE_BLKS);
-        int nt = tb % 72, kt = tb / 72;
-        int n0 = nt*64, k0 = kt*64;
-        for (int p = 0; p < 16; p++) {
-            int idx = t + 256*p;
-            int kk = idx >> 6, nn = idx & 63;
-            lds[nn*66 + kk] = __float2half(rw2[(k0+kk)*WNUM + n0+nn]);
-        }
-        __syncthreads();
-        for (int p = 0; p < 16; p++) {
-            int idx = t + 256*p;
-            int nn = idx >> 6, kk = idx & 63;
-            rw2T[(n0+nn)*HID + k0+kk] = lds[nn*66 + kk];
-        }
-    } else {
-        for (int p = 0; p < 6; p++) inv[t + 256*p] = -1;
-        for (int p = 0; p < 4; p++) {
-            int e = t + 256*p;
-            float d = att_dist[e];
-            envE[e] = (d < CUTOFF) ? 0.5f*(cosf(3.14159265358979323846f*d/CUTOFF) + 1.0f) : 0.0f;
-            float vx = att_vec[3*e], vy = att_vec[3*e+1], vz = att_vec[3*e+2];
-            float nrm = sqrtf(vx*vx + vy*vy + vz*vz);
-            float is = 1.0f / fmaxf(nrm, 1e-8f);
-            const float s3 = 1.7320508075688772f;
-            y1E[3*e]   = s3*vx*is;
-            y1E[3*e+1] = s3*vy*is;
-            y1E[3*e+2] = s3*vz*is;
-        }
-        __syncthreads();
-        for (int p = 0; p < 4; p++) { int e = t + 256*p; inv[att_dst[e]] = e; }
-    }
-}
-
-__global__ __launch_bounds__(256) void k_mq(
-    const __half* __restrict__ hiddenH, const __half* __restrict__ rw2T,
-    const float* __restrict__ rb2,
-    const float* __restrict__ habs1, const float* __restrict__ ec, const float* __restrict__ qb1,
-    const float* __restrict__ qw2, const float* __restrict__ qb2,
-    const float* __restrict__ qw3, const float* __restrict__ qb3,
-    __half* __restrict__ tpwE, float* __restrict__ qmat)
-{
-    __shared__ __align__(16) char smemraw[17408];
-    int blk = blockIdx.x;
-    int t = threadIdx.x;
-    if (blk < MFMA_BLKS) {
-        int colTile = blk % 36;
-        int rowGrp  = blk / 36;
-        int wv = t >> 6;
-        int lane = t & 63;
-        int m0 = (rowGrp*4 + wv) * 16;
-        int n0 = colTile * 128;
-        int mrow = lane & 15, quad = lane >> 4;
-        __half* cS = (__half*)smemraw + wv * (16*136);
-        const _Float16* hp = (const _Float16*)hiddenH + (m0 + mrow)*HID + quad*8;
-        half8_t af[4];
-        #pragma unroll
-        for (int kc = 0; kc < 4; kc++) af[kc] = *(const half8_t*)(hp + kc*32);
-        #pragma unroll
-        for (int nt = 0; nt < 8; nt++) {
-            const _Float16* bp = (const _Float16*)rw2T + (n0 + nt*16 + mrow)*HID + quad*8;
-            float4v acc = {0.f, 0.f, 0.f, 0.f};
-            #pragma unroll
-            for (int kc = 0; kc < 4; kc++) {
-                half8_t bf = *(const half8_t*)(bp + kc*32);
-                acc = __builtin_amdgcn_mfma_f32_16x16x32_f16(af[kc], bf, acc, 0, 0, 0);
-            }
-            float bias = rb2[n0 + nt*16 + mrow];
-            #pragma unroll
-            for (int r = 0; r < 4; r++)
-                cS[(quad*4 + r)*136 + nt*16 + mrow] = __float2half(acc[r] + bias);
-        }
-        #pragma unroll
-        for (int p = 0; p < 4; p++) {
-            int chunk = lane + 64*p;
-            int row = chunk >> 4, c8 = (chunk & 15)*8;
-            float4 v = *(float4*)&cS[row*136 + c8];
-            *(float4*)&tpwE[(long)(m0 + row)*WNUM + n0 + c8] = v;
-        }
-    } else {
-        float* l1S = (float*)smemraw;
-        float* l2S = (float*)smemraw + 1024;
-        int r0 = (blk - MFMA_BLKS) * 8;
-        for (int p = 0; p < 4; p++) {
-            int idx = t + 256*p;
-            int rr = idx >> 7, i = idx & 127;
-            int be = r0 + rr; int b = be >> 8; int e = be & 255;
-            l1S[rr*128 + i] = silu_f(habs1[b*HID + i] + ec[e*HID + i] + qb1[i]);
-        }
-        __syncthreads();
+            for (int n = 0; n < NN; n++) {
+                float a = aS[el][n];
+                float4 v = *(const float4*)&vp[n*OUT_DIM];
+                acc.x += a*v.x; acc.y += a*v.y; acc.z += a*v.z; acc.w += a*v.w;
+            }
+            float4 g = *(float4*)&gS[el][c4*4];
+            float4 o; o.x = acc.x*g.x; o.y = acc.y*g.y; o.z = acc.z*g.z; o.w = acc.w*g.w;
+            *(float4*)&ocS[el][c4*4] = o;
+        }
+        __syncthreads();
+
+        for (int uu = t; uu < 8*INVD; uu += 256) {
+            int el = uu / INVD, j = uu - INVD*(uu/INVD);
+            float val;
+            if (j < M0O) val = ocS[el][j];
+            else {
+                int o = j - M0O;
+                float x = ocS[el][M0O + 3*o], y = ocS[el][M0O + 3*o + 1], zz = ocS[el][M0O + 3*o + 2];
+                val = sqrtf(x*x + y*y + zz*zz + 1e-12f);
+            }
+            inS[el][j] = val;
+        }
+        __syncthreads();
+
         int r = t >> 5, c0 = (t & 31)*4;
         {
-            float4 a0 = *(const float4*)&qb2[c0];
+            float4 a0 = *(const float4*)&ob1[c0];
+            float4 a1 = make_float4(0,0,0,0);
+            #pragma unroll 8
+            for (int i = 0; i < INVD; i += 2) {
+                float x0v = inS[r][i], x1v = inS[r][i+1];
+                float4 w0 = *(const float4*)&ow1[i*HID + c0];
+                float4 w1 = *(const float4*)&ow1[(i+1)*HID + c0];
+                a0.x += x0v*w0.x; a0.y += x0v*w0.y; a0.z += x0v*w0.z; a0.w += x0v*w0.w;
+                a1.x += x1v*w1.x; a1.y += x1v*w1.y; a1.z += x1v*w1.z; a1.w += x1v*w1.w;
+            }
+            l1S[r][c0]   = silu_f(a0.x + a1.x); l1S[r][c0+1] = silu_f(a0.y + a1.y);
+            l1S[r][c0+2] = silu_f(a0.z + a1.z); l1S[r][c0+3] = silu_f(a0.w + a1.w);
+        }
+        __syncthreads();
+        {
+            float4 a0 = *(const float4*)&ob2[c0];
             float4 a1 = make_float4(0,0,0,0);
             #pragma unroll 8
             for (int i = 0; i < HID; i += 2) {
-                float x0v = l1S[r*128 + i], x1v = l1S[r*128 + i+1];
-                float4 w0 = *(const float4*)&qw2[i*HID + c0];
-                float4 w1 = *(const float4*)&qw2[(i+1)*HID + c0];
+                float x0v = l1S[r][i], x1v = l1S[r][i+1];
+                float4 w0 = *(const float4*)&ow2[i*HID + c0];
+                float4 w1 = *(const float4*)&ow2[(i+1)*HID + c0];
                 a0.x += x0v*w0.x; a0.y += x0v*w0.y; a0.z += x0v*w0.z; a0.w += x0v*w0.w;
                 a1.x += x1v*w1.x; a1.y += x1v*w1.y; a1.z += x1v*w1.z; a1.w += x1v*w1.w;
             }
-            l2S[r*128 + c0]   = silu_f(a0.x + a1.x); l2S[r*128 + c0+1] = silu_f(a0.y + a1.y);
-            l2S[r*128 + c0+2] = silu_f(a0.z + a1.z); l2S[r*128 + c0+3] = silu_f(a0.w + a1.w);
+            l2S[r][c0]   = silu_f(a0.x + a1.x); l2S[r][c0+1] = silu_f(a0.y + a1.y);
+            l2S[r][c0+2] = silu_f(a0.z + a1.z); l2S[r][c0+3] = silu_f(a0.w + a1.w);
         }
         __syncthreads();
         {
-            float4 a0 = *(const float4*)&qb3[c0];
+            float4 a0 = *(const float4*)&ob3[c0];
             float4 a1 = make_float4(0,0,0,0);
             #pragma unroll 8
             for (int i = 0; i < HID; i += 2) {
-                float x0v = l2S[r*128 + i], x1v = l2S[r*128 + i+1];
-                float4 w0 = *(const float4*)&qw3[i*HID + c0];
-                float4 w1 = *(const float4*)&qw3[(i+1)*HID + c0];
+                float x0v = l2S[r][i], x1v = l2S[r][i+1];
+                float4 w0 = *(const float4*)&ow3[i*HID + c0];
+                float4 w1 = *(const float4*)&ow3[(i+1)*HID + c0];
                 a0.x += x0v*w0.x; a0.y += x0v*w0.y; a0.z += x0v*w0.z; a0.w += x0v*w0.w;
                 a1.x += x1v*w1.x; a1.y += x1v*w1.y; a1.z += x1v*w1.z; a1.w += x1v*w1.w;
             }
             float4 o;
             o.x = a0.x + a1.x; o.y = a0.y + a1.y; o.z = a0.z + a1.z; o.w = a0.w + a1.w;
-            *(float4*)&qmat[(r0 + r)*LAT + c0] = o;
-        }
-    }
-}
-
-__global__ __launch_bounds__(256) void k_st(
-    const float* __restrict__ qmat, const float* __restrict__ kmat, const int* __restrict__ inv,
-    const float* __restrict__ h_full, const __half* __restrict__ tpwE,
-    const int* __restrict__ att_dst,
-    const float* __restrict__ envE, const float* __restrict__ y1E,
-    float* __restrict__ scoresW, float* __restrict__ virr)
-{
-    __shared__ float smem[8544];
-    int blk = blockIdx.x;
-    int t = threadIdx.x;
-    if (blk < SCORE_BLKS) {
-        int b  = blk >> 3;
-        int e0 = (blk & 7) * 32;
-        float (*Qs)[132] = (float(*)[132])smem;
-        float (*Kt)[132] = (float(*)[132])(smem + 32*132);
-        float* mS = smem + 2*32*132;
-        for (int p = 0; p < 4; p++) {
-            int idx = t + 256*p; int e = idx >> 5, i4 = idx & 31;
-            *(float4*)&Qs[e][i4*4] = *(const float4*)&qmat[(b*NE + e0 + e)*LAT + i4*4];
-        }
-        if (t < NN) mS[t] = ((unsigned)inv[b*NN + t] < E_ATT) ? 1.0f : 0.0f;
-        int te = t >> 5, tn = t & 31;
-        float acc[4][3] = {};
-        for (int nt = 0; nt < 3; nt++) {
-            __syncthreads();
-            for (int p = 0; p < 4; p++) {
-                int idx = t + 256*p; int n = idx >> 5, i4 = idx & 31;
-                *(float4*)&Kt[n][i4*4] = *(const float4*)&kmat[(b*NN + nt*32 + n)*LAT + i4*4];
-            }
-            __syncthreads();
-            for (int i = 0; i < LAT; i++) {
-                float bv = Kt[tn][i];
-                acc[0][nt] += Qs[te*4 + 0][i]*bv;
-                acc[1][nt] += Qs[te*4 + 1][i]*bv;
-                acc[2][nt] += Qs[te*4 + 2][i]*bv;
-                acc[3][nt] += Qs[te*4 + 3][i]*bv;
-            }
-        }
-        const float scale = 0.04419417382415922f;
-        #pragma unroll
-        for (int j = 0; j < 4; j++)
-            #pragma unroll
-            for (int jj = 0; jj < 3; jj++) {
-                int n = tn + 32*jj;
-                float s = (mS[n] != 0.f) ? acc[j][jj]*scale : -1e9f;
-                scoresW[((b*NE) + e0 + te*4 + j)*NN + n] = s;
-            }
-    } else {
-        int sub = t >> 7, tt = t & 127;
-        int e = (blk - SCORE_BLKS)*2 + sub;
-        int f = att_dst[e];
-        float* x0  = smem + sub*256;
-        float* x1f = smem + sub*256 + 64;
-        float* xy  = smem + sub*256 + 160;
-        float* y1s = smem + sub*256 + 192;
-        const float* hf = h_full + f*NODE_DIM;
-        if (tt < M0I) x0[tt] = hf[tt];
-        if (tt < M1I*3) x1f[tt] = hf[M0I + tt];
-        if (tt < 3) y1s[tt] = y1E[3*e + tt];
-        __syncthreads();
-        if (tt < M1I) xy[tt] = x1f[3*tt]*y1s[0] + x1f[3*tt+1]*y1s[1] + x1f[3*tt+2]*y1s[2];
-        __syncthreads();
-        float scale = envE[e];
-        const __half* w = tpwE + (long)e*WNUM;
-        const float alpha = 0.10206207261596575f;
-        const float cc = 0.5773502691896258f;
-        if (tt < M0O) {
-            float t00 = 0.f, t11 = 0.f;
-            #pragma unroll 4
-            for (int i = 0; i < M0I; i++) t00 += x0[i]*__half2float(w[i*M0O + tt]);
-            #pragma unroll 4
-            for (int i = 0; i < M1I; i++) t11 += xy[i]*__half2float(w[SEG3 + i*M0O + tt]);
-            virr[f*OUT_DIM + tt] = alpha*(t00 + cc*t11)*scale;
-        } else if (tt < M0O + 3*M1O) {
-            int idx = tt - M0O; int o = idx/3, m = idx - 3*o;
-            float t01 = 0.f, t10 = 0.f;
-            #pragma unroll 4
-            for (int i = 0; i < M0I; i++) t01 += x0[i]*__half2float(w[SEG1 + i*M1O + o]);
-            #pragma unroll 4
-            for (int i = 0; i < M1I; i++) t10 += x1f[i*3 + m]*__half2float(w[SEG2 + i*M1O + o]);
-            virr[f*OUT_DIM + tt] = alpha*cc*(t01*y1s[m] + t10)*scale;
-        }
-    }
-}
-
-__global__ __launch_bounds__(256) void k_attf(
-    const float* __restrict__ scoresW, const int* __restrict__ inv,
-    const float* __restrict__ virr, const float* __restrict__ gexp,
-    const float* __restrict__ ow1, const float* __restrict__ ob1,
-    const float* __restrict__ ow2, const float* __restrict__ ob2,
-    const float* __restrict__ ow3, const float* __restrict__ ob3,
-    float* __restrict__ out)
-{
-    int b  = blockIdx.x >> 5;
-    int e0 = (blockIdx.x & 31) * 8;
-    int t = threadIdx.x;
-    __shared__ float aS[8][100];
-    __shared__ float gS[8][84];
-    __shared__ float ocS[8][84];
-    __shared__ float mS[NN];
-    __shared__ float inS[8][INVD];
-    __shared__ float l1S[8][HID];
-    __shared__ float l2S[8][HID];
-
-    for (int p = 0; p < 3; p++) {
-        int idx = t + 256*p;
-        int el = idx / NN, n = idx - NN*(idx/NN);
-        aS[el][n] = scoresW[((b*NE) + e0 + el)*NN + n];
-    }
-    if (t < 160) {
-        int el = t / 20, c4 = t - 20*(t/20);
-        *(float4*)&gS[el][c4*4] = *(const float4*)&gexp[(e0 + el)*OUT_DIM + c4*4];
-    }
-    if (t < NN) mS[t] = ((unsigned)inv[b*NN + t] < E_ATT) ? 1.0f : 0.0f;
-    __syncthreads();
-
-    {
-        int el = t >> 5;
-        int ng = t & 31;
-        float s0 = aS[el][ng], s1 = aS[el][ng + 32], s2 = aS[el][ng + 64];
-        float m0 = mS[ng], m1 = mS[ng + 32], m2 = mS[ng + 64];
-        float mx = fmaxf(s0, fmaxf(s1, s2));
-        #pragma unroll
-        for (int off = 1; off < 32; off <<= 1) mx = fmaxf(mx, __shfl_xor(mx, off));
-        float e0v = expf(s0 - mx), e1v = expf(s1 - mx), e2v = expf(s2 - mx);
-        float sm = e0v + e1v + e2v;
-        #pragma unroll
-        for (int off = 1; off < 32; off <<= 1) sm += __shfl_xor(sm, off);
-        float r = 1.0f / sm;
-        float p0 = m0*e0v*r, p1 = m1*e1v*r, p2 = m2*e2v*r;
-        float ss = p0 + p1 + p2;
-        #pragma unroll
-        for (int off = 1; off < 32; off <<= 1) ss += __shfl_xor(ss, off);
-        float is = 1.0f / fmaxf(ss, 1e-8f);
-        aS[el][ng]      = p0*is;
-        aS[el][ng + 32] = p1*is;
-        aS[el][ng + 64] = p2*is;
-    }
-    __syncthreads();
-
-    if (t < 160) {
-        int el = t / 20, c4 = t - 20*(t/20);
-        const float* vp = virr + (long)b*NN*OUT_DIM + c4*4;
-        float4 acc = make_float4(0,0,0,0);
-        #pragma unroll 4
-        for (int n = 0; n < NN; n++) {
-            float a = aS[el][n];
-            float4 v = *(const float4*)&vp[n*OUT_DIM];
-            acc.x += a*v.x; acc.y += a*v.y; acc.z += a*v.z; acc.w += a*v.w;
-        }
-        float4 g = *(float4*)&gS[el][c4*4];
-        float4 o; o.x = acc.x*g.x; o.y = acc.y*g.y; o.z = acc.z*g.z; o.w = acc.w*g.w;
-        *(float4*)&ocS[el][c4*4] = o;
-    }
-    __syncthreads();
-
-    for (int u = t; u < 8*INVD; u += 256) {
-        int el = u / INVD, j = u - INVD*(u/INVD);
-        float val;
-        if (j < M0O) val = ocS[el][j];
-        else {
-            int o = j - M0O;
-            float x = ocS[el][M0O + 3*o], y = ocS[el][M0O + 3*o + 1], zz = ocS[el][M0O + 3*o + 2];
-            val = sqrtf(x*x + y*y + zz*zz + 1e-12f);
-        }
-        inS[el][j] = val;
-    }
-    __syncthreads();
-
-    int r = t >> 5, c0 = (t & 31)*4;
-    {
-        float4 a0 = *(const float4*)&ob1[c0];
-        float4 a1 = make_float4(0,0,0,0);
-        #pragma unroll 8
-        for (int i = 0; i < INVD; i += 2) {
-            float x0v = inS[r][i], x1v = inS[r][i+1];
-            float4 w0 = *(const float4*)&ow1[i*HID + c0];
-            float4 w1 = *(const float4*)&ow1[(i+1)*HID + c0];
-            a0.x += x0v*w0.x; a0.y += x0v*w0.y; a0.z += x0v*w0.z; a0.w += x0v*w0.w;
-            a1.x += x1v*w1.x; a1.y += x1v*w1.y; a1.z += x1v*w1.z; a1.w += x1v*w1.w;
-        }
-        l1S[r][c0]   = silu_f(a0.x + a1.x); l1S[r][c0+1] = silu_f(a0.y + a1.y);
-        l1S[r][c0+2] = silu_f(a0.z + a1.z); l1S[r][c0+3] = silu_f(a0.w + a1.w);
-    }
-    __syncthreads();
-    {
-        float4 a0 = *(const float4*)&ob2[c0];
-        float4 a1 = make_float4(0,0,0,0);
-        #pragma unroll 8
-        for (int i = 0; i < HID; i += 2) {
-            float x0v = l1S[r][i], x1v = l1S[r][i+1];
-            float4 w0 = *(const float4*)&ow2[i*HID + c0];
-            float4 w1 = *(const float4*)&ow2[(i+1)*HID + c0];
-            a0.x += x0v*w0.x; a0.y += x0v*w0.y; a0.z += x0v*w0.z; a0.w += x0v*w0.w;
-            a1.x += x1v*w1.x; a1.y += x1v*w1.y; a1.z += x1v*w1.z; a1.w += x1v*w1.w;
-        }
-        l2S[r][c0]   = silu_f(a0.x + a1.x); l2S[r][c0+1] = silu_f(a0.y + a1.y);
-        l2S[r][c0+2] = silu_f(a0.z + a1.z); l2S[r][c0+3] = silu_f(a0.w + a1.w);
-    }
-    __syncthreads();
-    {
-        float4 a0 = *(const float4*)&ob3[c0];
-        float4 a1 = make_float4(0,0,0,0);
-        #pragma unroll 8
-        for (int i = 0; i < HID; i += 2) {
-            float x0v = l2S[r][i], x1v = l2S[r][i+1];
-            float4 w0 = *(const float4*)&ow3[i*HID + c0];
-            float4 w1 = *(const float4*)&ow3[(i+1)*HID + c0];
-            a0.x += x0v*w0.x; a0.y += x0v*w0.y; a0.z += x0v*w0.z; a0.w += x0v*w0.w;
-            a1.x += x1v*w1.x; a1.y += x1v*w1.y; a1.z += x1v*w1.z; a1.w += x1v*w1.w;
-        }
-        float4 o;
-        o.x = a0.x + a1.x; o.y = a0.y + a1.y; o.z = a0.z + a1.z; o.w = a0.w + a1.w;
-        *(float4*)&out[((b*NE + e0) + r)*LAT + c0] = o;
+            *(float4*)&out[((b*NE + e0) + r)*LAT + c0] = o;
+        }
     }
 }
 
 extern "C" void kernel_launch(void* const* d_in, const int* in_sizes, int n_in,
                               void* d_out, int out_size, void* d_ws, size_t ws_size,
                               hipStream_t stream) {
-    const float* h        = (const float*)d_in[0];
-    const float* h_full   = (const float*)d_in[1];
-    const float* e_feat   = (const float*)d_in[2];
-    const float* att_dist = (const float*)d_in[3];
-    const float* att_vec  = (const float*)d_in[4];
-    const float* z_emb    = (const float*)d_in[5];
-    const float* rw1 = (const float*)d_in[6];  const float* rb1 = (const float*)d_in[7];
-    const float* rw2 = (const float*)d_in[8];  const float* rb2 = (const float*)d_in[9];
-    const float* ew1 = (const float*)d_in[10]; const float* eb1 = (const float*)d_in[11];
-    const float* ew2 = (const float*)d_in[12]; const float* eb2 = (const float*)d_in[13];
-    const float* qw1 = (const float*)d_in[14]; const float* qb1 = (const float*)d_in[15];
-    const float* qw2 = (const float*)d_in[16]; const float* qb2 = (const float*)d_in[17];
-    const float* qw3 = (const float*)d_in[18]; const float* qb3 = (const float*)d_in[19];
-    const float* kw1 = (const float*)d_in[20]; const float* kb1 = (const float*)d_in[21];
-    const float* kw2 = (const float*)d_in[22]; const float* kb2 = (const float*)d_in[23];
-    const float* kw3 = (const float*)d_in[24]; const float* kb3 = (const float*)d_in[25];
-    const float* ow1 = (const float*)d_in[26]; const float* ob1 = (const float*)d_in[27];
-    const float* ow2 = (const float*)d_in[28]; const float* ob2 = (const float*)d_in[29];
-    const float* ow3 = (const float*)d_in[30]; const float* ob3 = (const float*)d_in[31];
-    const int* z        = (const int*)d_in[32];
-    const int* absorber = (const int*)d_in[34];
-    const int* att_dst  = (const int*)d_in[35];
+    Params prm;
+    prm.h        = (const float*)d_in[0];
+    prm.h_full   = (const float*)d_in[1];
+    prm.e_feat   = (const float*)d_in[2];
+    prm.att_dist = (const float*)d_in[3];
+    prm.att_vec  = (const float*)d_in[4];
+    prm.z_emb    = (const float*)d_in[5];
+    prm.rw1 = (const float*)d_in[6];  prm.rb1 = (const float*)d_in[7];
+    prm.rw2 = (const float*)d_in[8];  prm.rb2 = (const float*)d_in[9];
+    prm.ew1 = (const float*)d_in[10]; prm.eb1 = (const float*)d_in[11];
+    prm.ew2 = (const float*)d_in[12]; prm.eb2 = (const float*)d_in[13];
+    prm.qw1 = (const float*)d_in[14]; prm.qb1 = (const float*)d_in[15];
+    prm.qw2 = (const float*)d_in[16]; prm.qb2 = (const float*)d_in[17];
+    prm.qw3 = (const float*)d_in[18]; prm.qb3 = (const float*)d_in[19];
+    prm.kw1 = (const float*)d_in[20]; prm.kb1 = (const float*)d_in[21];
+    prm.kw2 = (const float*)d_in[22]; prm.kb2 = (const float*)d_in[23];
+    prm.kw3 = (const float*)d_in[24]; prm.kb3 = (const float*)d_in[25];
+    prm.ow1 = (const float*)d_in[26]; prm.ob1 = (const float*)d_in[27];
+    prm.ow2 = (const float*)d_in[28]; prm.ob2 = (const float*)d_in[29];
+    prm.ow3 = (const float*)d_in[30]; prm.ob3 = (const float*)d_in[31];
+    prm.z        = (const int*)d_in[32];
+    prm.absorber = (const int*)d_in[34];
+    prm.att_dst  = (const int*)d_in[35];
 
     float* ws = (float*)d_ws;
-    int*   inv     = (int*)ws;
-    float* y1E     = ws + 1536;
-    float* envE    = ws + 4608;
-    float* kmat    = ws + 5632;
-    float* qmat    = ws + 202240;
-    float* gexp    = ws + 726528;
-    float* virr    = ws + 747008;
-    float* habs1   = ws + 869888;
-    float* ec      = ws + 871936;
-    float* scoresW = ws + 904704;
-    __half* tpwE   = (__half*)(ws + 1297920);
-    __half* rw2T   = (__half*)(ws + 3657216);
-    __half* hiddenH= (__half*)(ws + 3952128);
-
-    float* out = (float*)d_out;
-
-    k_stage1<<<STAGE1_BLKS, 256, 0, stream>>>(h, z_emb, z, absorber, e_feat,
-                                              att_dst, att_dist, att_vec,
-                                              rw1, rb1, kw1, kb1, kw2, kb2, kw3, kb3,
-                                              qw1, ew1, eb1, ew2, eb2, rw2,
-                                              hiddenH, kmat, ec, habs1, gexp, rw2T,
-                                              inv, y1E, envE);
-    k_mq<<<MQ_BLKS, 256, 0, stream>>>(hiddenH, rw2T, rb2, habs1, ec, qb1,
-                                      qw2, qb2, qw3, qb3, tpwE, qmat);
-    k_st<<<ST_BLKS, 256, 0, stream>>>(qmat, kmat, inv, h_full, tpwE, att_dst,
-                                      envE, y1E, scoresW, virr);
-    k_attf<<<BB*32, 256, 0, stream>>>(scoresW, inv, virr, gexp,
-                                      ow1, ob1, ow2, ob2, ow3, ob3, out);
+    prm.inv     = (int*)ws;
+    prm.y1E     = ws + 1536;
+    prm.envE    = ws + 4608;
+    prm.kmat    = ws + 5632;
+    prm.qmat    = ws + 202240;
+    prm.gexp    = ws + 726528;
+    prm.virr    = ws + 747008;
+    prm.habs1   = ws + 869888;
+    prm.ec      = ws + 871936;
+    prm.scoresW = ws + 904704;
+    prm.tpwE    = (__half*)(ws + 1297920);
+    prm.rw2T    = (__half*)(ws + 3657216);
+    prm.hiddenH = (__half*)(ws + 3952128);
+    prm.bar     = (int*)(ws + 4100096);
+
+    prm.out = (float*)d_out;
+
+    k_init<<<1, 64, 0, stream>>>(prm.bar);
+    k_mega<<<GRID_BLKS, 256, 0, stream>>>(prm);
 }
```
